# Performance work log

Measured on AMD Instinct MI355X. Metric: run time of the kernel, lower is better.

Reference implementation:

```python
import jax, jax.numpy as jnp
import numpy as np

B, K, S = 4096, 32, 6          # batch, n_neighbors, n_shifts
QD, H, NH = 512, 384, 6        # query_dim, hidden_dim, n_heads
HD = H // NH                   # head_dim
NR = 20                        # n_residue_types (table has NR+1 rows)
NBR_IN = S + S + 16 + 1 + 1    # neighbor_proj input dim = 30

def gelu(x):
    return jax.nn.gelu(x, approximate=False)

def setup_inputs():
    key = jax.random.key(0)
    ks = iter(jax.random.split(key, 64))
    def nrm(shape, scale=0.05):
        return jax.random.normal(next(ks), shape, dtype=jnp.float32) * scale
    inp = {}
    inp['query_encoding'] = jax.random.normal(next(ks), (B, QD), dtype=jnp.float32)
    inp['query_residue_code'] = jax.random.randint(next(ks), (B,), 0, NR + 1).astype(jnp.int32)
    inp['query_observed_shifts'] = jax.random.normal(next(ks), (B, S), dtype=jnp.float32)
    inp['query_shift_masks'] = (jax.random.uniform(next(ks), (B, S)) < 0.8).astype(jnp.float32)
    inp['retrieved_shifts'] = jax.random.normal(next(ks), (B, K, S), dtype=jnp.float32)
    inp['retrieved_shift_masks'] = jax.random.uniform(next(ks), (B, K, S)) < 0.8
    inp['retrieved_residue_codes'] = jax.random.randint(next(ks), (B, K), 0, NR + 1).astype(jnp.int32)
    inp['retrieved_distances'] = jax.random.uniform(next(ks), (B, K), dtype=jnp.float32)
    inp['retrieved_valid'] = jax.random.uniform(next(ks), (B, K)) < 0.9
    # parameters (buffers + weights). rc_table kept finite (no NaN rows sampled).
    inp['rc_table'] = nrm((NR + 1, S), 1.0)
    inp['W_qp'] = nrm((QD, H)); inp['b_qp'] = jnp.zeros((H,))
    inp['E_res'] = nrm((NR + 1, 16))
    inp['W_np'] = nrm((NBR_IN, H)); inp['b_np'] = jnp.zeros((H,))
    inp['W_aq'] = nrm((H, H)); inp['b_aq'] = jnp.zeros((H,))
    inp['W_ak'] = nrm((H, H)); inp['b_ak'] = jnp.zeros((H,))
    inp['W_av'] = nrm((H, H)); inp['b_av'] = jnp.zeros((H,))
    inp['W_ss1'] = nrm((2 * S, H // 2)); inp['b_ss1'] = jnp.zeros((H // 2,))
    inp['W_ss2'] = nrm((H // 2, NH)); inp['b_ss2'] = jnp.zeros((NH,))
    inp['W_cp1'] = nrm((H, H)); inp['b_cp1'] = jnp.zeros((H,))
    inp['W_cp2'] = nrm((H, H)); inp['b_cp2'] = jnp.zeros((H,))
    inp['W_sw1'] = nrm((H, H)); inp['b_sw1'] = jnp.zeros((H,))
    inp['W_sw2'] = nrm((H, S)); inp['b_sw2'] = jnp.zeros((S,))
    inp['E_trust'] = nrm((NR + 1, 32))
    inp['W_tq'] = nrm((QD, H)); inp['b_tq'] = jnp.zeros((H,))
    inp['W_tc'] = nrm((H + 32 + 4, H)); inp['b_tc'] = jnp.zeros((H,))
    inp['W_tp1'] = nrm((H + 4, H // 2)); inp['b_tp1'] = jnp.zeros((H // 2,))
    inp['W_tp2'] = nrm((H // 2, 1)); inp['b_tp2'] = jnp.zeros((1,))
    inp['shift_scale'] = jnp.ones((S,)); inp['fallback_shift'] = jnp.zeros((S,))
    inp['fallback_context'] = jnp.zeros((H,))
    return inp

def _forward(p):
    eps = 1e-8
    qcode = p['query_residue_code']; rcodes = p['retrieved_residue_codes']
    smask = p['retrieved_shift_masks']; valid = p['retrieved_valid']
    dist = p['retrieved_distances']; rc = p['rc_table']
    # --- RC correction: corrected = RC[query] + (shift - RC[retrieved]) ---
    qidx = jnp.clip(qcode, 0, rc.shape[0] - 1)
    ridx = jnp.clip(rcodes, 0, rc.shape[0] - 1)
    rc_q = rc[qidx][:, None, :]            # (B,1,S)
    rc_r = rc[ridx]                         # (B,K,S)
    corrected = rc_q + (p['retrieved_shifts'] - rc_r)
    rc_valid = (~jnp.isnan(rc_q)) & (~jnp.isnan(rc_r))
    corrected = jnp.where(rc_valid, corrected, p['retrieved_shifts'])
    shifts = jnp.where(smask, corrected, p['retrieved_shifts'])  # (B,K,S)
    any_valid = valid.any(axis=1)                                # (B,)
    same_type = (rcodes == qcode[:, None]).astype(jnp.float32)   # (B,K)
    # --- projections ---
    q = gelu(p['query_encoding'] @ p['W_qp'] + p['b_qp'])        # (B,H)
    res_emb = p['E_res'][rcodes]                                 # (B,K,16)
    nbr = jnp.concatenate([shifts, smask.astype(jnp.float32), res_emb,
                           dist[..., None], same_type[..., None]], axis=-1)
    kv = gelu(nbr @ p['W_np'] + p['b_np'])                       # (B,K,H)
    # --- multi-head cross attention (single query token) ---
    Qh = (q @ p['W_aq'] + p['b_aq']).reshape(B, NH, HD)
    Kh = (kv @ p['W_ak'] + p['b_ak']).reshape(B, K, NH, HD)
    Vh = (kv @ p['W_av'] + p['b_av']).reshape(B, K, NH, HD)
    scores = jnp.einsum('bhd,bkhd->bhk', Qh, Kh) * (HD ** -0.5)  # (B,NH,K)
    sdiff = jnp.concatenate([
        (p['query_observed_shifts'][:, None, :] - shifts) * p['query_shift_masks'][:, None, :],
        jnp.broadcast_to(p['query_shift_masks'][:, None, :], (B, K, S))], axis=-1)
    bias = gelu(sdiff @ p['W_ss1'] + p['b_ss1']) @ p['W_ss2'] + p['b_ss2']  # (B,K,NH)
    scores = scores + jnp.transpose(bias, (0, 2, 1))
    # if nothing valid, unmask slot 0 (matches torch all_masked fixup)
    valid_eff = valid | ((~any_valid)[:, None] & (jnp.arange(K) == 0)[None, :])
    scores = jnp.where(valid_eff[:, None, :], scores, -10000.0)
    w = jax.nn.softmax(scores, axis=-1)
    attn_out = jnp.einsum('bhk,bkhd->bhd', w, Vh).reshape(B, H)
    ctx = gelu(attn_out @ p['W_cp1'] + p['b_cp1']) @ p['W_cp2'] + p['b_cp2']
    ctx = jnp.where(any_valid[:, None], ctx, p['fallback_context'][None, :])
    # --- shift transfer ---
    swb = gelu(attn_out @ p['W_sw1'] + p['b_sw1']) @ p['W_sw2'] + p['b_sw2']  # (B,S)
    weights = dist[..., None] + same_type[..., None] * 0.5 + swb[:, None, :] * 0.1  # (B,K,S)
    valid_mask = valid[..., None] & smask
    weights = jnp.where(valid_mask, weights, -10000.0)
    weights = jax.nn.softmax(weights, axis=1)
    transferred = jnp.sum(weights * shifts, axis=1) * p['shift_scale']
    transferred = jnp.where(any_valid[:, None], transferred, p['fallback_shift'][None, :])
    # --- trust statistics (no grad in original) ---
    vm = valid_mask.astype(jnp.float32)
    cnt = vm.sum(axis=1)                                         # (B,S)
    cov = cnt / (K + eps)
    mean = (shifts * vm).sum(axis=1) / (cnt + eps)
    var = (((shifts - mean[:, None, :]) ** 2) * vm).sum(axis=1) / (cnt + eps)
    var_n = jnp.clip(jnp.log1p(var), 0.0, 5.0) / 5.0
    mdist = (dist[..., None] * vm).sum(axis=1) / (cnt + eps)
    stp = (same_type[..., None] * vm).sum(axis=1) / (cnt + eps)
    per_stats = jax.lax.stop_gradient(jnp.stack([cov, var_n, mdist, stp], axis=-1))  # (B,S,4)
    vf = valid.astype(jnp.float32)
    n_valid = vf.sum(axis=1, keepdims=True) / K
    n_same = (same_type * vf).sum(axis=1, keepdims=True) / K
    dmask = jnp.where(valid, dist, 0.0)
    gmean = dmask.sum(axis=1, keepdims=True) / (vf.sum(axis=1, keepdims=True) + eps)
    gmax = dmask.max(axis=1, keepdims=True)
    gstats = jax.lax.stop_gradient(jnp.concatenate([gmean, gmax, n_valid, n_same], axis=-1))  # (B,4)
    # --- trust head ---
    qre = p['E_trust'][qcode]                                    # (B,32)
    tq = gelu(p['query_encoding'] @ p['W_tq'] + p['b_tq'])
    tc = gelu(jnp.concatenate([tq, qre, gstats], axis=-1) @ p['W_tc'] + p['b_tc'])  # (B,H)
    tin = jnp.concatenate([jnp.broadcast_to(tc[:, None, :], (B, S, H)), per_stats], axis=-1)
    trust = jax.nn.sigmoid(gelu(tin @ p['W_tp1'] + p['b_tp1']) @ p['W_tp2'] + p['b_tp2'])[..., 0]
    return ctx, transferred, trust

def reference(query_encoding, query_residue_code, query_observed_shifts, query_shift_masks,
              retrieved_shifts, retrieved_shift_masks, retrieved_residue_codes,
              retrieved_distances, retrieved_valid, rc_table,
              W_qp, b_qp, E_res, W_np, b_np, W_aq, b_aq, W_ak, b_ak, W_av, b_av,
              W_ss1, b_ss1, W_ss2, b_ss2, W_cp1, b_cp1, W_cp2, b_cp2,
              W_sw1, b_sw1, W_sw2, b_sw2, E_trust, W_tq, b_tq, W_tc, b_tc,
              W_tp1, b_tp1, W_tp2, b_tp2, shift_scale, fallback_shift, fallback_context):
    return _forward(dict(locals()))
```

## Files before the change

kernel.cpp:

```cpp
#include <hip/hip_runtime.h>

typedef unsigned short u16;
typedef unsigned int u32;
typedef __attribute__((ext_vector_type(8))) short bf16x8;
typedef __attribute__((ext_vector_type(4))) float f32x4;

__device__ __forceinline__ float fs(float f) {
    return (f == f && fabsf(f) < 1e30f) ? f : 0.f;
}
__device__ __forceinline__ float fin(float v) {
    return (v == v && fabsf(v) < 1e30f) ? v : 555.0f;
}
__device__ __forceinline__ u16 f2b(float f) {
    union { float f; unsigned int i; } w; w.f = f;
    unsigned int r = w.i + 0x7FFFu + ((w.i >> 16) & 1u);
    return (u16)(r >> 16);
}
__device__ __forceinline__ float b2f(u16 b) {
    union { unsigned int i; float f; } w; w.i = ((unsigned int)b) << 16;
    return w.f;
}
__device__ __forceinline__ float gelu_f(float x) {
    return 0.5f * x * (1.0f + erff(x * 0.70710678118654752440f));
}

__global__ void fill_kernel(float* __restrict__ out, int n, float val) {
    int i = blockIdx.x * 256 + threadIdx.x;
    if (i < n) out[i] = val;
}

struct CvtSrcs { const float* p[14]; };

__global__ void k_cvt_all(CvtSrcs sp, u16* __restrict__ w) {
    int id = blockIdx.x * 256 + threadIdx.x;
    if (id >= 3640448) return;
    if (id < 2097152) { w[id] = f2b(fs(sp.p[0][id])); return; }
    if (id >= 2637824 && id < 2785280) { w[id] = f2b(fs(sp.p[4][id - 2637824])); return; }
    const float* src; int local, K, N, Kp;
    if (id < 2293760)      { src = sp.p[1];  local = id - 2097152; K = 512; N = 384; Kp = 512; }
    else if (id < 2490368) { src = sp.p[2];  local = id - 2293760; K = 512; N = 384; Kp = 512; }
    else if (id < 2637824) { src = sp.p[3];  local = id - 2490368; K = 384; N = 384; Kp = 384; }
    else if (id < 2932736) { src = sp.p[5];  local = id - 2785280; K = 384; N = 384; Kp = 384; }
    else if (id < 3080192) { src = sp.p[6];  local = id - 2932736; K = 384; N = 384; Kp = 384; }
    else if (id < 3227648) { src = sp.p[7];  local = id - 3080192; K = 384; N = 384; Kp = 384; }
    else if (id < 3375104) { src = sp.p[8];  local = id - 3227648; K = 384; N = 384; Kp = 384; }
    else if (id < 3547136) { src = sp.p[9];  local = id - 3375104; K = 420; N = 384; Kp = 448; }
    else if (id < 3620864) { src = sp.p[10]; local = id - 3547136; K = 384; N = 192; Kp = 384; }
    else if (id < 3633152) { src = sp.p[11]; local = id - 3620864; K = 30;  N = 384; Kp = 32;  }
    else if (id < 3634304) { src = sp.p[12]; local = id - 3633152; K = 192; N = 6;   Kp = 192; }
    else                   { src = sp.p[13]; local = id - 3634304; K = 12;  N = 192; Kp = 32;  }
    int n = local / Kp, k = local - n * Kp;
    w[id] = (k < K) ? f2b(fs(src[(size_t)k * N + n])) : (u16)0;
}

__global__ void k_prep(const float* __restrict__ rshift, const int* __restrict__ rsmask,
                       const int* __restrict__ qcode, const int* __restrict__ rcodes,
                       const float* __restrict__ rdist, const float* __restrict__ rc_table,
                       const float* __restrict__ E_res,
                       float* __restrict__ nbr, int NBc)
{
    int gk = blockIdx.x * 256 + threadIdx.x;
    if (gk >= NBc) return;
    int b = gk >> 5;
    int qc = qcode[b], rc = rcodes[gk];
    int qi = min(max(qc, 0), 20), ri = min(max(rc, 0), 20);
    float dist = fs(rdist[gk]);
    float same = (rc == qc) ? 1.f : 0.f;
    float* nr = nbr + (size_t)gk * 30;
    for (int s = 0; s < 6; s++) {
        float rs = fs(rshift[gk * 6 + s]);
        bool m = rsmask[gk * 6 + s] != 0;
        float rq = rc_table[qi * 6 + s];
        float rr = rc_table[ri * 6 + s];
        bool rcv = (rq == rq) && (rr == rr) && fabsf(rq) < 1e30f && fabsf(rr) < 1e30f;
        float sh = (m && rcv) ? (rq + rs - rr) : rs;
        nr[s] = sh;
        nr[6 + s] = m ? 1.f : 0.f;
    }
    for (int j = 0; j < 16; j++) nr[12 + j] = fs(E_res[ri * 16 + j]);
    nr[28] = dist;
    nr[29] = same;
}

__global__ void k_stats_w(const float* __restrict__ nbr, const int* __restrict__ rvalid,
                          float* __restrict__ pst, float* __restrict__ gst,
                          float* __restrict__ anyv, int BCc)
{
    int wid = (blockIdx.x * 256 + threadIdx.x) >> 6;
    int lane = threadIdx.x & 63;
    if (wid >= BCc * 4) return;
    int b = wid >> 2, sub = wid & 3;
    if (sub < 3) {
        int s = sub * 2 + (lane >> 5), k = lane & 31;
        const float* nr = nbr + (size_t)(b * 32 + k) * 30;
        float vf = (rvalid[b * 32 + k] != 0) ? 1.f : 0.f;
        float vm = vf * nr[6 + s];
        float shv = nr[s], dist = nr[28], same = nr[29];
        float cnt = vm, msum = shv * vm, mdist = dist * vm, mst = same * vm;
#pragma unroll
        for (int m = 1; m <= 16; m <<= 1) {
            cnt += __shfl_xor(cnt, m);
            msum += __shfl_xor(msum, m);
            mdist += __shfl_xor(mdist, m);
            mst += __shfl_xor(mst, m);
        }
        float inv = 1.f / (cnt + 1e-8f);
        float mean = msum * inv;
        float dv = shv - mean;
        float var = dv * dv * vm;
#pragma unroll
        for (int m = 1; m <= 16; m <<= 1) var += __shfl_xor(var, m);
        var *= inv;
        if (k == 0) {
            float* p = pst + (size_t)b * 24 + s * 4;
            p[0] = cnt * (1.f / 32.f);
            p[1] = fminf(fmaxf(log1pf(var), 0.f), 5.f) * 0.2f;
            p[2] = mdist * inv;
            p[3] = mst * inv;
        }
    } else {
        int k = lane & 31;
        float svf = 0.f, sdm = 0.f, mdm = -1e30f, ssm = 0.f;
        if (lane < 32) {
            const float* nr = nbr + (size_t)(b * 32 + k) * 30;
            float vf = (rvalid[b * 32 + k] != 0) ? 1.f : 0.f;
            float dm = vf * nr[28];
            svf = vf; sdm = dm; mdm = dm; ssm = vf * nr[29];
        }
#pragma unroll
        for (int m = 1; m <= 32; m <<= 1) {
            svf += __shfl_xor(svf, m);
            sdm += __shfl_xor(sdm, m);
            mdm = fmaxf(mdm, __shfl_xor(mdm, m));
            ssm += __shfl_xor(ssm, m);
        }
        if (lane == 0) {
            float* g = gst + (size_t)b * 4;
            g[0] = sdm / (svf + 1e-8f);
            g[1] = mdm;
            g[2] = svf * (1.f / 32.f);
            g[3] = ssm * (1.f / 32.f);
            anyv[b] = (svf > 0.f) ? 1.f : 0.f;
        }
    }
}

template <int ACT, bool OUTF, bool OUTB>
__device__ __forceinline__ void gemm_body128(
    const u16* __restrict__ A, int lda,
    const u16* __restrict__ BT, int ldb,
    const float* __restrict__ bias, const float* __restrict__ bias1,
    float* __restrict__ Cf, u16* __restrict__ Cb, int ldc,
    int K, int m0, int n0)
{
    __shared__ u16 As[128 * 72];
    __shared__ u16 Bs[64 * 72];
    const int t = threadIdx.x;
    const int lane = t & 63, wave = t >> 6;
    const int wm = (wave & 1) << 6, wn = (wave >> 1) << 5;
    const int frm = lane & 15, frq = lane >> 4;
    const int r0 = t >> 3, c0 = (t & 7) << 3;
    const f32x4 z = {0.f, 0.f, 0.f, 0.f};
    f32x4 acc[4][2] = {{z, z}, {z, z}, {z, z}, {z, z}};
    for (int k0 = 0; k0 < K; k0 += 64) {
#pragma unroll
        for (int i = 0; i < 4; i++)
            *(bf16x8*)&As[(r0 + 32 * i) * 72 + c0] =
                *(const bf16x8*)&A[(size_t)(m0 + r0 + 32 * i) * lda + k0 + c0];
#pragma unroll
        for (int i = 0; i < 2; i++)
            *(bf16x8*)&Bs[(r0 + 32 * i) * 72 + c0] =
                *(const bf16x8*)&BT[(size_t)(n0 + r0 + 32 * i) * ldb + k0 + c0];
        __syncthreads();
#pragma unroll
        for (int kk = 0; kk < 2; kk++) {
            const int fo = (kk << 5) + (frq << 3);
            bf16x8 b0 = *(const bf16x8*)&Bs[(wn + frm) * 72 + fo];
            bf16x8 b1 = *(const bf16x8*)&Bs[(wn + 16 + frm) * 72 + fo];
#pragma unroll
            for (int mi = 0; mi < 4; mi++) {
                bf16x8 a = *(const bf16x8*)&As[(wm + (mi << 4) + frm) * 72 + fo];
                acc[mi][0] = __builtin_amdgcn_mfma_f32_16x16x32_bf16(a, b0, acc[mi][0], 0, 0, 0);
                acc[mi][1] = __builtin_amdgcn_mfma_f32_16x16x32_bf16(a, b1, acc[mi][1], 0, 0, 0);
            }
        }
        __syncthreads();
    }
#pragma unroll
    for (int mi = 0; mi < 4; mi++) {
#pragma unroll
        for (int ni = 0; ni < 2; ni++) {
            int col = n0 + wn + (ni << 4) + frm;
            float bv = 0.f;
            if (bias) {
                if (bias1 && col >= 384) bv = fs(bias1[col - 384]);
                else bv = fs(bias[col]);
            }
#pragma unroll
            for (int r = 0; r < 4; r++) {
                int row = m0 + wm + (mi << 4) + (frq << 2) + r;
                float v = acc[mi][ni][r] + bv;
                if (ACT == 1) v = gelu_f(v);
                if (OUTF) Cf[(size_t)row * ldc + col] = v;
                if (OUTB) Cb[(size_t)row * ldc + col] = f2b(v);
            }
        }
    }
}

template <int ACT, bool OUTF, bool OUTB>
__global__ __launch_bounds__(256) void k_gemm_bb(
    const u16* __restrict__ A, int lda, const u16* __restrict__ BT, int ldb,
    const float* __restrict__ bias, float* __restrict__ Cf, u16* __restrict__ Cb,
    int ldc, int K)
{
    gemm_body128<ACT, OUTF, OUTB>(A, lda, BT, ldb, bias, nullptr, Cf, Cb, ldc, K,
                                  blockIdx.y << 7, blockIdx.x << 6);
}

template <int ACT>
__global__ __launch_bounds__(256) void k_gemm_bb2(
    const u16* __restrict__ A, int lda, const u16* __restrict__ BT, int ldb,
    const float* __restrict__ bias0, const float* __restrict__ bias1,
    u16* __restrict__ Cb, int ldc, int K)
{
    gemm_body128<ACT, false, true>(A, lda, BT, ldb, bias0, bias1, nullptr, Cb, ldc, K,
                                   blockIdx.y << 7, blockIdx.x << 6);
}

__global__ __launch_bounds__(256) void k_gemm_ctx(
    const u16* __restrict__ A, int lda, const u16* __restrict__ BT, int ldb,
    const float* __restrict__ bias, const float* __restrict__ anyv,
    const float* __restrict__ fctx, float* __restrict__ outp, int ldc, int K)
{
    __shared__ u16 As[128 * 72];
    __shared__ u16 Bs[64 * 72];
    const int t = threadIdx.x;
    const int lane = t & 63, wave = t >> 6;
    const int m0 = blockIdx.y << 7, n0 = blockIdx.x << 6;
    const int wm = (wave & 1) << 6, wn = (wave >> 1) << 5;
    const int frm = lane & 15, frq = lane >> 4;
    const int r0 = t >> 3, c0 = (t & 7) << 3;
    const f32x4 z = {0.f, 0.f, 0.f, 0.f};
    f32x4 acc[4][2] = {{z, z}, {z, z}, {z, z}, {z, z}};
    for (int k0 = 0; k0 < K; k0 += 64) {
#pragma unroll
        for (int i = 0; i < 4; i++)
            *(bf16x8*)&As[(r0 + 32 * i) * 72 + c0] =
                *(const bf16x8*)&A[(size_t)(m0 + r0 + 32 * i) * lda + k0 + c0];
#pragma unroll
        for (int i = 0; i < 2; i++)
            *(bf16x8*)&Bs[(r0 + 32 * i) * 72 + c0] =
                *(const bf16x8*)&BT[(size_t)(n0 + r0 + 32 * i) * ldb + k0 + c0];
        __syncthreads();
#pragma unroll
        for (int kk = 0; kk < 2; kk++) {
            const int fo = (kk << 5) + (frq << 3);
            bf16x8 b0 = *(const bf16x8*)&Bs[(wn + frm) * 72 + fo];
            bf16x8 b1 = *(const bf16x8*)&Bs[(wn + 16 + frm) * 72 + fo];
#pragma unroll
            for (int mi = 0; mi < 4; mi++) {
                bf16x8 a = *(const bf16x8*)&As[(wm + (mi << 4) + frm) * 72 + fo];
                acc[mi][0] = __builtin_amdgcn_mfma_f32_16x16x32_bf16(a, b0, acc[mi][0], 0, 0, 0);
                acc[mi][1] = __builtin_amdgcn_mfma_f32_16x16x32_bf16(a, b1, acc[mi][1], 0, 0, 0);
            }
        }
        __syncthreads();
    }
#pragma unroll
    for (int mi = 0; mi < 4; mi++) {
#pragma unroll
        for (int ni = 0; ni < 2; ni++) {
            int col = n0 + wn + (ni << 4) + frm;
            float bv = fs(bias[col]);
            float fv = fs(fctx[col]);
#pragma unroll
            for (int r = 0; r < 4; r++) {
                int row = m0 + wm + (mi << 4) + (frq << 2) + r;
                float v = acc[mi][ni][r] + bv;
                v = (anyv[row] > 0.f) ? v : fv;
                outp[(size_t)row * ldc + col] = fin(v);
            }
        }
    }
}

__global__ __launch_bounds__(256) void k_gemm_tc(
    const u16* __restrict__ qtqb, const int* __restrict__ qcode,
    const float* __restrict__ Etr, const float* __restrict__ gst,
    const u16* __restrict__ BT, const float* __restrict__ bias,
    u16* __restrict__ Cb)
{
    __shared__ u16 As[128 * 72];
    __shared__ u16 Bs[64 * 72];
    const int t = threadIdx.x;
    const int lane = t & 63, wave = t >> 6;
    const int m0 = blockIdx.y << 7, n0 = blockIdx.x << 6;
    const int wm = (wave & 1) << 6, wn = (wave >> 1) << 5;
    const int frm = lane & 15, frq = lane >> 4;
    const int r0 = t >> 3, c0 = (t & 7) << 3;
    const f32x4 z = {0.f, 0.f, 0.f, 0.f};
    f32x4 acc[4][2] = {{z, z}, {z, z}, {z, z}, {z, z}};
    for (int k0 = 0; k0 < 448; k0 += 64) {
        if (k0 < 384) {
#pragma unroll
            for (int i = 0; i < 4; i++)
                *(bf16x8*)&As[(r0 + 32 * i) * 72 + c0] =
                    *(const bf16x8*)&qtqb[(size_t)(m0 + r0 + 32 * i) * 768 + 384 + k0 + c0];
        } else {
#pragma unroll
            for (int i = 0; i < 4; i++) {
                int row = m0 + r0 + 32 * i;
                int qi = min(max(qcode[row], 0), 20);
#pragma unroll
                for (int j = 0; j < 8; j++) {
                    int col = k0 + c0 + j;
                    u16 v;
                    if (col < 416) v = f2b(fs(Etr[qi * 32 + (col - 384)]));
                    else if (col < 420) v = f2b(gst[(size_t)row * 4 + (col - 416)]);
                    else v = (u16)0;
                    As[(r0 + 32 * i) * 72 + c0 + j] = v;
                }
            }
        }
#pragma unroll
        for (int i = 0; i < 2; i++)
            *(bf16x8*)&Bs[(r0 + 32 * i) * 72 + c0] =
                *(const bf16x8*)&BT[(size_t)(n0 + r0 + 32 * i) * 448 + k0 + c0];
        __syncthreads();
#pragma unroll
        for (int kk = 0; kk < 2; kk++) {
            const int fo = (kk << 5) + (frq << 3);
            bf16x8 b0 = *(const bf16x8*)&Bs[(wn + frm) * 72 + fo];
            bf16x8 b1 = *(const bf16x8*)&Bs[(wn + 16 + frm) * 72 + fo];
#pragma unroll
            for (int mi = 0; mi < 4; mi++) {
                bf16x8 a = *(const bf16x8*)&As[(wm + (mi << 4) + frm) * 72 + fo];
                acc[mi][0] = __builtin_amdgcn_mfma_f32_16x16x32_bf16(a, b0, acc[mi][0], 0, 0, 0);
                acc[mi][1] = __builtin_amdgcn_mfma_f32_16x16x32_bf16(a, b1, acc[mi][1], 0, 0, 0);
            }
        }
        __syncthreads();
    }
#pragma unroll
    for (int mi = 0; mi < 4; mi++) {
#pragma unroll
        for (int ni = 0; ni < 2; ni++) {
            int col = n0 + wn + (ni << 4) + frm;
            float bv = fs(bias[col]);
#pragma unroll
            for (int r = 0; r < 4; r++) {
                int row = m0 + wm + (mi << 4) + (frq << 2) + r;
                Cb[(size_t)row * 384 + col] = f2b(gelu_f(acc[mi][ni][r] + bv));
            }
        }
    }
}

__global__ __launch_bounds__(256) void k_qp_loop(
    const u16* __restrict__ Qhb, const u16* __restrict__ WakB,
    const float* __restrict__ bak, u16* __restrict__ Qpb, float* __restrict__ qkb)
{
    __shared__ u16 As[64 * 72];
    __shared__ u16 Bs[64 * 72];
    const int t = threadIdx.x;
    const int lane = t & 63, wave = t >> 6;
    const int m0 = blockIdx.x << 6, hd = blockIdx.y;
    const int wm = (wave & 1) << 5, wn = (wave >> 1) << 5;
    const int frm = lane & 15, frq = lane >> 4;
    const int r0 = t >> 3, c0 = (t & 7) << 3;
    const f32x4 z = {0.f, 0.f, 0.f, 0.f};
    *(bf16x8*)&As[r0 * 72 + c0]        = *(const bf16x8*)&Qhb[(size_t)(m0 + r0) * 384 + hd * 64 + c0];
    *(bf16x8*)&As[(r0 + 32) * 72 + c0] = *(const bf16x8*)&Qhb[(size_t)(m0 + r0 + 32) * 384 + hd * 64 + c0];
    __syncthreads();
    {
        int r = t >> 2, p = t & 3;
        float acc = 0.f;
#pragma unroll
        for (int i = 0; i < 16; i++) {
            int d = p * 16 + i;
            acc += b2f(As[r * 72 + d]) * fs(bak[hd * 64 + d]);
        }
        acc += __shfl_xor(acc, 1);
        acc += __shfl_xor(acc, 2);
        if (p == 0) qkb[(m0 + r) * 6 + hd] = acc;
    }
    for (int nt = 0; nt < 6; nt++) {
        *(bf16x8*)&Bs[r0 * 72 + c0]        = *(const bf16x8*)&WakB[(size_t)(nt * 64 + r0) * 384 + hd * 64 + c0];
        *(bf16x8*)&Bs[(r0 + 32) * 72 + c0] = *(const bf16x8*)&WakB[(size_t)(nt * 64 + r0 + 32) * 384 + hd * 64 + c0];
        __syncthreads();
        f32x4 acc[2][2] = {{z, z}, {z, z}};
#pragma unroll
        for (int kk = 0; kk < 2; kk++) {
            const int fo = (kk << 5) + (frq << 3);
            bf16x8 a0 = *(const bf16x8*)&As[(wm + frm) * 72 + fo];
            bf16x8 a1 = *(const bf16x8*)&As[(wm + 16 + frm) * 72 + fo];
            bf16x8 b0 = *(const bf16x8*)&Bs[(wn + frm) * 72 + fo];
            bf16x8 b1 = *(const bf16x8*)&Bs[(wn + 16 + frm) * 72 + fo];
            acc[0][0] = __builtin_amdgcn_mfma_f32_16x16x32_bf16(a0, b0, acc[0][0], 0, 0, 0);
            acc[0][1] = __builtin_amdgcn_mfma_f32_16x16x32_bf16(a0, b1, acc[0][1], 0, 0, 0);
            acc[1][0] = __builtin_amdgcn_mfma_f32_16x16x32_bf16(a1, b0, acc[1][0], 0, 0, 0);
            acc[1][1] = __builtin_amdgcn_mfma_f32_16x16x32_bf16(a1, b1, acc[1][1], 0, 0, 0);
        }
#pragma unroll
        for (int mi = 0; mi < 2; mi++) {
#pragma unroll
            for (int ni = 0; ni < 2; ni++) {
                int col = nt * 64 + wn + (ni << 4) + frm;
#pragma unroll
                for (int r = 0; r < 4; r++) {
                    int row = m0 + wm + (mi << 4) + (frq << 2) + r;
                    Qpb[(size_t)row * 2304 + hd * 384 + col] = f2b(acc[mi][ni][r]);
                }
            }
        }
        __syncthreads();
    }
}

__global__ __launch_bounds__(256) void k_attnout_bb(
    const u16* __restrict__ vmsb, const u16* __restrict__ WavT,
    const float* __restrict__ bav, u16* __restrict__ attnb)
{
    int hd = blockIdx.x;
    gemm_body128<0, false, true>(vmsb + hd * 384, 2304, WavT + (size_t)hd * 64 * 384, 384,
                                 bav + hd * 64, nullptr, nullptr, attnb + hd * 64, 384, 384,
                                 blockIdx.y << 7, 0);
}

__global__ __launch_bounds__(384) void k_attnblk(
    const float* __restrict__ nbr, const u16* __restrict__ WnpT,
    const float* __restrict__ bnp, const u16* __restrict__ Qpb,
    const float* __restrict__ qkb,
    const float* __restrict__ qobs, const float* __restrict__ qmask,
    const u16* __restrict__ Wss1T, const float* __restrict__ bss1,
    const u16* __restrict__ Wss2T, const float* __restrict__ bss2,
    const int* __restrict__ rvalid, const float* __restrict__ anyv,
    u16* __restrict__ vmsb)
{
    __shared__ u16 kvsb[32 * 392];
    __shared__ u16 qSb[6 * 392];
    __shared__ u16 hidSb[32 * 200];
    __shared__ u16 sdS[32 * 32];
    __shared__ float wsx[192];
    __shared__ float bsS[32 * 8];
    __shared__ float uSf[512];
    u16* aS = (u16*)uSf;
    float* sS = uSf;
    const int b = blockIdx.x;
    const int t = threadIdx.x;
    const int lane = t & 63, wave = t >> 6;
    const int frm = lane & 15, frq = lane >> 4;
    for (int i = t; i < 1152; i += 384) {
        int h = i / 192, k2 = i - h * 192;
        ((u32*)qSb)[h * 196 + k2] = ((const u32*)(Qpb + (size_t)b * 2304))[i];
    }
    {
        const float* nr = nbr + (size_t)b * 960;
        for (int i = t; i < 1024; i += 384) {
            int r = i >> 5, cc = i & 31;
            aS[r * 32 + cc] = (cc < 30) ? f2b(nr[r * 30 + cc]) : (u16)0;
        }
        if (t < 32) {
            const float* nr2 = nr + t * 30;
#pragma unroll
            for (int s = 0; s < 6; s++) {
                float qm = fs(qmask[b * 6 + s]);
                sdS[t * 32 + s] = f2b((fs(qobs[b * 6 + s]) - nr2[s]) * qm);
                sdS[t * 32 + 6 + s] = f2b(qm);
            }
#pragma unroll
            for (int j = 12; j < 32; j++) sdS[t * 32 + j] = (u16)0;
        }
    }
    __syncthreads();
    {
        bf16x8 a0 = *(const bf16x8*)&aS[frm * 32 + (frq << 3)];
        bf16x8 a1 = *(const bf16x8*)&aS[(16 + frm) * 32 + (frq << 3)];
        const f32x4 z = {0.f, 0.f, 0.f, 0.f};
        f32x4 acc0[4] = {z, z, z, z};
        f32x4 acc1[4] = {z, z, z, z};
#pragma unroll
        for (int ct = 0; ct < 4; ct++) {
            int col = (wave << 6) + (ct << 4) + frm;
            bf16x8 bf = *(const bf16x8*)&WnpT[col * 32 + (frq << 3)];
            acc0[ct] = __builtin_amdgcn_mfma_f32_16x16x32_bf16(a0, bf, acc0[ct], 0, 0, 0);
            acc1[ct] = __builtin_amdgcn_mfma_f32_16x16x32_bf16(a1, bf, acc1[ct], 0, 0, 0);
        }
#pragma unroll
        for (int ct = 0; ct < 4; ct++) {
            int col = (wave << 6) + (ct << 4) + frm;
            float bb = fs(bnp[col]);
#pragma unroll
            for (int r = 0; r < 4; r++) {
                int row0 = (frq << 2) + r;
                kvsb[row0 * 392 + col] = f2b(gelu_f(acc0[ct][r] + bb));
                kvsb[(row0 + 16) * 392 + col] = f2b(gelu_f(acc1[ct][r] + bb));
            }
        }
        bf16x8 sa0 = *(const bf16x8*)&sdS[frm * 32 + (frq << 3)];
        bf16x8 sa1 = *(const bf16x8*)&sdS[(16 + frm) * 32 + (frq << 3)];
#pragma unroll
        for (int ct = 0; ct < 2; ct++) {
            int col = (wave << 5) + (ct << 4) + frm;
            bf16x8 bf = *(const bf16x8*)&Wss1T[col * 32 + (frq << 3)];
            f32x4 d0 = __builtin_amdgcn_mfma_f32_16x16x32_bf16(sa0, bf, z, 0, 0, 0);
            f32x4 d1 = __builtin_amdgcn_mfma_f32_16x16x32_bf16(sa1, bf, z, 0, 0, 0);
            float bb = fs(bss1[col]);
#pragma unroll
            for (int r = 0; r < 4; r++) {
                int k0r = (frq << 2) + r;
                hidSb[k0r * 200 + col] = f2b(gelu_f(d0[r] + bb));
                hidSb[(k0r + 16) * 200 + col] = f2b(gelu_f(d1[r] + bb));
            }
        }
    }
    __syncthreads();
    if (wave < 2) {
        f32x4 accs = {0.f, 0.f, 0.f, 0.f};
#pragma unroll
        for (int ks = 0; ks < 12; ks++) {
            bf16x8 af = *(const bf16x8*)&kvsb[((wave << 4) + frm) * 392 + (ks << 5) + (frq << 3)];
            int hh = (frm < 6) ? frm : 0;
            bf16x8 bf = *(const bf16x8*)&qSb[hh * 392 + (ks << 5) + (frq << 3)];
            accs = __builtin_amdgcn_mfma_f32_16x16x32_bf16(af, bf, accs, 0, 0, 0);
        }
        if (frm < 6) {
#pragma unroll
            for (int r = 0; r < 4; r++)
                sS[((wave << 4) + (frq << 2) + r) * 8 + frm] = accs[r];
        }
    } else if (wave < 4) {
        int w2 = wave - 2;
        f32x4 accb = {0.f, 0.f, 0.f, 0.f};
#pragma unroll
        for (int ks = 0; ks < 6; ks++) {
            bf16x8 a = *(const bf16x8*)&hidSb[((w2 << 4) + frm) * 200 + (ks << 5) + (frq << 3)];
            bf16x8 bf = *(const bf16x8*)&Wss2T[(frm < 6 ? frm : 0) * 192 + (ks << 5) + (frq << 3)];
            accb = __builtin_amdgcn_mfma_f32_16x16x32_bf16(a, bf, accb, 0, 0, 0);
        }
        if (frm < 6) {
            float bb = fs(bss2[frm]);
#pragma unroll
            for (int r = 0; r < 4; r++)
                bsS[((w2 << 4) + (frq << 2) + r) * 8 + frm] = accb[r] + bb;
        }
    }
    __syncthreads();
    if (t < 192) {
        int h = t >> 5, k = t & 31;
        float s = (sS[k * 8 + h] + qkb[b * 6 + h]) * 0.125f + bsS[k * 8 + h];
        bool ve = (rvalid[b * 32 + k] != 0) || (anyv[b] == 0.f && k == 0);
        s = ve ? s : -10000.f;
        float mx = s;
        mx = fmaxf(mx, __shfl_xor(mx, 1));
        mx = fmaxf(mx, __shfl_xor(mx, 2));
        mx = fmaxf(mx, __shfl_xor(mx, 4));
        mx = fmaxf(mx, __shfl_xor(mx, 8));
        mx = fmaxf(mx, __shfl_xor(mx, 16));
        float e = expf(s - mx);
        float sum = e;
        sum += __shfl_xor(sum, 1);
        sum += __shfl_xor(sum, 2);
        sum += __shfl_xor(sum, 4);
        sum += __shfl_xor(sum, 8);
        sum += __shfl_xor(sum, 16);
        wsx[h * 32 + k] = e / sum;
    }
    __syncthreads();
    {
        float a0 = 0.f, a1 = 0.f, a2 = 0.f, a3 = 0.f, a4 = 0.f, a5 = 0.f;
        for (int k = 0; k < 32; k++) {
            float kvv = b2f(kvsb[k * 392 + t]);
            a0 += wsx[k] * kvv;
            a1 += wsx[32 + k] * kvv;
            a2 += wsx[64 + k] * kvv;
            a3 += wsx[96 + k] * kvv;
            a4 += wsx[128 + k] * kvv;
            a5 += wsx[160 + k] * kvv;
        }
        u16* vp = vmsb + (size_t)b * 2304;
        vp[t] = f2b(a0);
        vp[384 + t] = f2b(a1);
        vp[768 + t] = f2b(a2);
        vp[1152 + t] = f2b(a3);
        vp[1536 + t] = f2b(a4);
        vp[1920 + t] = f2b(a5);
    }
}

__global__ void k_swb_w(const u16* __restrict__ hs1b, const float* __restrict__ Wsw2,
                        const float* __restrict__ bsw2, float* __restrict__ swb, int BCc)
{
    int wid = (blockIdx.x * 256 + threadIdx.x) >> 6;
    int lane = threadIdx.x & 63;
    if (wid >= BCc * 6) return;
    int b = wid / 6, s = wid - b * 6;
    float acc = 0.f;
#pragma unroll
    for (int i = 0; i < 6; i++) {
        int n = lane + 64 * i;
        acc += b2f(hs1b[(size_t)b * 768 + 384 + n]) * fs(Wsw2[n * 6 + s]);
    }
#pragma unroll
    for (int m = 1; m <= 32; m <<= 1) acc += __shfl_xor(acc, m);
    if (lane == 0) swb[b * 6 + s] = acc + fs(bsw2[s]);
}

__global__ void k_tail_w(const float* __restrict__ tcp, const float* __restrict__ pst,
                         const float* __restrict__ Wtp1, const float* __restrict__ Wtp2,
                         const float* __restrict__ btp2, float* __restrict__ outT,
                         const float* __restrict__ nbr, const int* __restrict__ rsmask,
                         const int* __restrict__ rvalid, const float* __restrict__ swb,
                         const float* __restrict__ anyv, const float* __restrict__ sscale,
                         const float* __restrict__ fshift, float* __restrict__ outX, int BCc)
{
    int wid = (blockIdx.x * 256 + threadIdx.x) >> 6;
    int lane = threadIdx.x & 63;
    if (wid >= BCc * 9) return;
    int b = wid / 9, sub = wid - b * 9;
    if (sub < 6) {
        int s = sub;
        const float* ps = pst + (size_t)b * 24 + s * 4;
        float p0 = ps[0], p1 = ps[1], p2 = ps[2], p3 = ps[3];
        float acc = 0.f;
#pragma unroll
        for (int i = 0; i < 3; i++) {
            int j = lane + 64 * i;
            float pre = tcp[(size_t)b * 192 + j];
            pre += p0 * fs(Wtp1[(size_t)384 * 192 + j]);
            pre += p1 * fs(Wtp1[(size_t)385 * 192 + j]);
            pre += p2 * fs(Wtp1[(size_t)386 * 192 + j]);
            pre += p3 * fs(Wtp1[(size_t)387 * 192 + j]);
            acc += gelu_f(pre) * fs(Wtp2[j]);
        }
#pragma unroll
        for (int m = 1; m <= 32; m <<= 1) acc += __shfl_xor(acc, m);
        if (lane == 0) {
            float tv = 1.f / (1.f + expf(-(acc + fs(btp2[0]))));
            outT[b * 6 + s] = fin(tv);
        }
    } else {
        int s2 = sub - 6;
        int s = s2 * 2 + (lane >> 5), k = lane & 31;
        if (anyv[b] <= 0.f) {
            if (k == 0) outX[b * 6 + s] = fin(fs(fshift[s]));
            return;
        }
        int gk = b * 32 + k;
        const float* nr = nbr + (size_t)gk * 30;
        float wb = swb[b * 6 + s] * 0.1f;
        bool m = (rvalid[gk] != 0) && (rsmask[gk * 6 + s] != 0);
        float wv = m ? (nr[28] + nr[29] * 0.5f + wb) : -10000.f;
        float mx = wv;
#pragma unroll
        for (int mm = 1; mm <= 16; mm <<= 1) mx = fmaxf(mx, __shfl_xor(mx, mm));
        float e = expf(wv - mx);
        float num = e * nr[s], den = e;
#pragma unroll
        for (int mm = 1; mm <= 16; mm <<= 1) {
            num += __shfl_xor(num, mm);
            den += __shfl_xor(den, mm);
        }
        if (k == 0) outX[b * 6 + s] = fin((num / den) * fs(sscale[s]));
    }
}

#define L1(total) <<<((total) + 255) / 256, 256, 0, stream>>>
#define LW(nwaves) <<<(((nwaves) * 64) + 255) / 256, 256, 0, stream>>>

extern "C" void kernel_launch(void* const* d_in, const int* in_sizes, int n_in,
                              void* d_out, int out_size, void* d_ws, size_t ws_size,
                              hipStream_t stream)
{
    float* out = (float*)d_out;

    static const int EXP[45] = {
        2097152, 4096, 24576, 24576, 786432, 786432, 131072, 131072, 131072, 126,
        196608, 384, 336, 11520, 384, 147456, 384, 147456, 384, 147456, 384,
        2304, 192, 1152, 6, 147456, 384, 147456, 384, 147456, 384, 2304, 6,
        672, 196608, 384, 161280, 384, 74496, 192, 192, 1, 6, 6, 384
    };
    if (n_in != 45) {
        fill_kernel L1(out_size)(out, out_size, 580.0f);
        return;
    }
    for (int i = 0; i < 45; i++) {
        if (in_sizes[i] != EXP[i]) {
            fill_kernel L1(out_size)(out, out_size, 600.0f + 4.0f * i);
            return;
        }
    }

    const float* i_qe    = (const float*)d_in[0];
    const int*   i_qcode = (const int*)d_in[1];
    const float* i_qobs  = (const float*)d_in[2];
    const float* i_qmask = (const float*)d_in[3];
    const float* i_rshift= (const float*)d_in[4];
    const int*   i_rsmask= (const int*)d_in[5];
    const int*   i_rcodes= (const int*)d_in[6];
    const float* i_rdist = (const float*)d_in[7];
    const int*   i_rvalid= (const int*)d_in[8];
    const float* i_rc    = (const float*)d_in[9];
    const float* i_Wqp   = (const float*)d_in[10];
    const float* i_bqp   = (const float*)d_in[11];
    const float* i_Eres  = (const float*)d_in[12];
    const float* i_Wnp   = (const float*)d_in[13];
    const float* i_bnp   = (const float*)d_in[14];
    const float* i_Waq   = (const float*)d_in[15];
    const float* i_baq   = (const float*)d_in[16];
    const float* i_Wak   = (const float*)d_in[17];
    const float* i_bak   = (const float*)d_in[18];
    const float* i_Wav   = (const float*)d_in[19];
    const float* i_bav   = (const float*)d_in[20];
    const float* i_Wss1  = (const float*)d_in[21];
    const float* i_bss1  = (const float*)d_in[22];
    const float* i_Wss2  = (const float*)d_in[23];
    const float* i_bss2  = (const float*)d_in[24];
    const float* i_Wcp1  = (const float*)d_in[25];
    const float* i_bcp1  = (const float*)d_in[26];
    const float* i_Wcp2  = (const float*)d_in[27];
    const float* i_bcp2  = (const float*)d_in[28];
    const float* i_Wsw1  = (const float*)d_in[29];
    const float* i_bsw1  = (const float*)d_in[30];
    const float* i_Wsw2  = (const float*)d_in[31];
    const float* i_bsw2  = (const float*)d_in[32];
    const float* i_Etr   = (const float*)d_in[33];
    const float* i_Wtq   = (const float*)d_in[34];
    const float* i_btq   = (const float*)d_in[35];
    const float* i_Wtc   = (const float*)d_in[36];
    const float* i_btc   = (const float*)d_in[37];
    const float* i_Wtp1  = (const float*)d_in[38];
    const float* i_btp1  = (const float*)d_in[39];
    const float* i_Wtp2  = (const float*)d_in[40];
    const float* i_btp2  = (const float*)d_in[41];
    const float* i_sscale= (const float*)d_in[42];
    const float* i_fshift= (const float*)d_in[43];
    const float* i_fctx  = (const float*)d_in[44];

    auto layoutBytes = [](int bc) -> size_t {
        auto al = [](size_t x) { return (x + 255) & ~(size_t)255; };
        size_t off = 0;
        off += al(3640448ull * 2);
        size_t nb = (size_t)bc * 32;
        off += al(nb * 30 * 4);
        off += al((size_t)bc * 192 * 4);
        off += al((size_t)bc * 2304 * 2) * 2;
        off += al((size_t)bc * 768 * 2) * 2;
        off += al((size_t)bc * 384 * 2) * 3;
        off += al((size_t)bc * 6 * 4) * 2 + al((size_t)bc * 24 * 4)
             + al((size_t)bc * 4 * 4) + al((size_t)bc * 4);
        return off;
    };
    const int cand[6] = {4096, 2048, 1024, 512, 256, 128};
    int BCc = 128;
    for (int i = 0; i < 6; i++) {
        if (layoutBytes(cand[i]) <= ws_size) { BCc = cand[i]; break; }
    }
    const int NBc = BCc * 32;

    char* wsb = (char*)d_ws;
    size_t off = 0;
    auto allocB = [&](size_t bytes) -> void* {
        void* p = (void*)(wsb + off);
        off = (off + bytes + 255) & ~(size_t)255;
        return p;
    };
    u16* wsW = (u16*)allocB(3640448ull * 2);
    u16* qeb   = wsW;
    u16* WqtqT = wsW + 2097152;
    u16* WaqT  = wsW + 2490368;
    u16* WakB  = wsW + 2637824;
    u16* WavT  = wsW + 2785280;
    u16* Wcp2T = wsW + 2932736;
    u16* Whs1T = wsW + 3080192;
    u16* WtcT  = wsW + 3375104;
    u16* Wtp1T = wsW + 3547136;
    u16* WnpT  = wsW + 3620864;
    u16* Wss2T = wsW + 3633152;
    u16* Wss1T = wsW + 3634304;
    float* nbr   = (float*)allocB((size_t)NBc * 30 * 4);
    float* tcpf  = (float*)allocB((size_t)BCc * 192 * 4);
    u16*   Qpb   = (u16*)allocB((size_t)BCc * 2304 * 2);
    u16*   vmsb  = (u16*)allocB((size_t)BCc * 2304 * 2);
    u16*   qtqb  = (u16*)allocB((size_t)BCc * 768 * 2);
    u16*   hs1b  = (u16*)allocB((size_t)BCc * 768 * 2);
    u16*   Qhb   = (u16*)allocB((size_t)BCc * 384 * 2);
    u16*   attnb = (u16*)allocB((size_t)BCc * 384 * 2);
    u16*   tcb   = (u16*)allocB((size_t)BCc * 384 * 2);
    float* swbf  = (float*)allocB((size_t)BCc * 6 * 4);
    float* qkbf  = (float*)allocB((size_t)BCc * 6 * 4);
    float* pstf  = (float*)allocB((size_t)BCc * 24 * 4);
    float* gstf  = (float*)allocB((size_t)BCc * 4 * 4);
    float* anyf  = (float*)allocB((size_t)BCc * 4);

    if (off > ws_size) {
        fill_kernel L1(out_size)(out, out_size, 1000.0f);
        return;
    }

    CvtSrcs sp;
    sp.p[0] = i_qe;  sp.p[1] = i_Wqp;  sp.p[2] = i_Wtq;  sp.p[3] = i_Waq;
    sp.p[4] = i_Wak; sp.p[5] = i_Wav;  sp.p[6] = i_Wcp2; sp.p[7] = i_Wcp1;
    sp.p[8] = i_Wsw1; sp.p[9] = i_Wtc; sp.p[10] = i_Wtp1; sp.p[11] = i_Wnp;
    sp.p[12] = i_Wss2; sp.p[13] = i_Wss1;
    k_cvt_all L1(3640448)(sp, wsW);

    for (int c = 0; c < 4096 / BCc; c++) {
        const size_t B0 = (size_t)c * BCc;
        const int MB = BCc / 128;
        const dim3 g6(6, MB), g3(3, MB), g12(12, MB), gao(6, MB);
        const dim3 gqp(BCc / 64, 6);
        k_prep L1(NBc)(i_rshift + B0 * 192, i_rsmask + B0 * 192, i_qcode + B0,
                       i_rcodes + B0 * 32, i_rdist + B0 * 32, i_rc, i_Eres, nbr, NBc);
        k_stats_w LW(BCc * 4)(nbr, i_rvalid + B0 * 32, pstf, gstf, anyf, BCc);
        k_gemm_bb2<1><<<g12, 256, 0, stream>>>(
            qeb + B0 * 512, 512, WqtqT, 512, i_bqp, i_btq, qtqb, 768, 512);
        k_gemm_bb<0, false, true><<<g6, 256, 0, stream>>>(
            qtqb, 768, WaqT, 384, i_baq, nullptr, Qhb, 384, 384);
        k_qp_loop<<<gqp, 256, 0, stream>>>(Qhb, WakB, i_bak, Qpb, qkbf);
        k_attnblk<<<BCc, 384, 0, stream>>>(nbr, WnpT, i_bnp, Qpb, qkbf,
                                           i_qobs + B0 * 6, i_qmask + B0 * 6,
                                           Wss1T, i_bss1, Wss2T, i_bss2,
                                           i_rvalid + B0 * 32, anyf, vmsb);
        k_attnout_bb<<<gao, 256, 0, stream>>>(vmsb, WavT, i_bav, attnb);
        k_gemm_bb2<1><<<g12, 256, 0, stream>>>(
            attnb, 384, Whs1T, 384, i_bcp1, i_bsw1, hs1b, 768, 384);
        k_gemm_ctx<<<g6, 256, 0, stream>>>(
            hs1b, 768, Wcp2T, 384, i_bcp2, anyf, i_fctx, out + B0 * 384, 384, 384);
        k_swb_w LW(BCc * 6)(hs1b, i_Wsw2, i_bsw2, swbf, BCc);
        k_gemm_tc<<<g6, 256, 0, stream>>>(
            qtqb, i_qcode + B0, i_Etr, gstf, WtcT, i_btc, tcb);
        k_gemm_bb<0, true, false><<<g3, 256, 0, stream>>>(
            tcb, 384, Wtp1T, 384, i_btp1, tcpf, nullptr, 192, 384);
        k_tail_w LW(BCc * 9)(tcpf, pstf, i_Wtp1, i_Wtp2, i_btp2,
                             out + (size_t)4096 * 390 + B0 * 6,
                             nbr, i_rsmask + B0 * 192, i_rvalid + B0 * 32, swbf, anyf,
                             i_sscale, i_fshift, out + (size_t)4096 * 384 + B0 * 6, BCc);
    }
}
```

Before: 394.2 us.

## Merge independent per-chunk kernels into combined launches and trim attention shared memory

```diff
diff --git a/kernel.cpp b/kernel.cpp
--- a/kernel.cpp
+++ b/kernel.cpp
@@ -53,14 +53,261 @@
     w[id] = (k < K) ? f2b(fs(src[(size_t)k * N + n])) : (u16)0;
 }
 
-__global__ void k_prep(const float* __restrict__ rshift, const int* __restrict__ rsmask,
-                       const int* __restrict__ qcode, const int* __restrict__ rcodes,
-                       const float* __restrict__ rdist, const float* __restrict__ rc_table,
-                       const float* __restrict__ E_res,
-                       float* __restrict__ nbr, int NBc)
-{
-    int gk = blockIdx.x * 256 + threadIdx.x;
-    if (gk >= NBc) return;
+
+template <int ACT, bool OUTF, bool OUTB>
+__device__ void gemm_body128(
+    u16* As, u16* Bs,
+    const u16* __restrict__ A, int lda,
+    const u16* __restrict__ BT, int ldb,
+    const float* __restrict__ bias, const float* __restrict__ bias1,
+    float* __restrict__ Cf, u16* __restrict__ Cb, int ldc,
+    int K, int m0, int n0)
+{
+    const int t = threadIdx.x;
+    const int lane = t & 63, wave = t >> 6;
+    const int wm = (wave & 1) << 6, wn = (wave >> 1) << 5;
+    const int frm = lane & 15, frq = lane >> 4;
+    const int r0 = t >> 3, c0 = (t & 7) << 3;
+    const f32x4 z = {0.f, 0.f, 0.f, 0.f};
+    f32x4 acc[4][2] = {{z, z}, {z, z}, {z, z}, {z, z}};
+    for (int k0 = 0; k0 < K; k0 += 64) {
+#pragma unroll
+        for (int i = 0; i < 4; i++)
+            *(bf16x8*)&As[(r0 + 32 * i) * 72 + c0] =
+                *(const bf16x8*)&A[(size_t)(m0 + r0 + 32 * i) * lda + k0 + c0];
+#pragma unroll
+        for (int i = 0; i < 2; i++)
+            *(bf16x8*)&Bs[(r0 + 32 * i) * 72 + c0] =
+                *(const bf16x8*)&BT[(size_t)(n0 + r0 + 32 * i) * ldb + k0 + c0];
+        __syncthreads();
+#pragma unroll
+        for (int kk = 0; kk < 2; kk++) {
+            const int fo = (kk << 5) + (frq << 3);
+            bf16x8 b0 = *(const bf16x8*)&Bs[(wn + frm) * 72 + fo];
+            bf16x8 b1 = *(const bf16x8*)&Bs[(wn + 16 + frm) * 72 + fo];
+#pragma unroll
+            for (int mi = 0; mi < 4; mi++) {
+                bf16x8 a = *(const bf16x8*)&As[(wm + (mi << 4) + frm) * 72 + fo];
+                acc[mi][0] = __builtin_amdgcn_mfma_f32_16x16x32_bf16(a, b0, acc[mi][0], 0, 0, 0);
+                acc[mi][1] = __builtin_amdgcn_mfma_f32_16x16x32_bf16(a, b1, acc[mi][1], 0, 0, 0);
+            }
+        }
+        __syncthreads();
+    }
+#pragma unroll
+    for (int mi = 0; mi < 4; mi++) {
+#pragma unroll
+        for (int ni = 0; ni < 2; ni++) {
+            int col = n0 + wn + (ni << 4) + frm;
+            float bv = 0.f;
+            if (bias) {
+                if (bias1 && col >= 384) bv = fs(bias1[col - 384]);
+                else bv = fs(bias[col]);
+            }
+#pragma unroll
+            for (int r = 0; r < 4; r++) {
+                int row = m0 + wm + (mi << 4) + (frq << 2) + r;
+                float v = acc[mi][ni][r] + bv;
+                if (ACT == 1) v = gelu_f(v);
+                if (OUTF) Cf[(size_t)row * ldc + col] = v;
+                if (OUTB) Cb[(size_t)row * ldc + col] = f2b(v);
+            }
+        }
+    }
+}
+
+__device__ void gemm_ctx_body(
+    u16* As, u16* Bs,
+    const u16* __restrict__ A, const u16* __restrict__ BT,
+    const float* __restrict__ bias, const float* __restrict__ anyv,
+    const float* __restrict__ fctx, float* __restrict__ outp,
+    int m0, int n0)
+{
+    const int t = threadIdx.x;
+    const int lane = t & 63, wave = t >> 6;
+    const int wm = (wave & 1) << 6, wn = (wave >> 1) << 5;
+    const int frm = lane & 15, frq = lane >> 4;
+    const int r0 = t >> 3, c0 = (t & 7) << 3;
+    const f32x4 z = {0.f, 0.f, 0.f, 0.f};
+    f32x4 acc[4][2] = {{z, z}, {z, z}, {z, z}, {z, z}};
+    for (int k0 = 0; k0 < 384; k0 += 64) {
+#pragma unroll
+        for (int i = 0; i < 4; i++)
+            *(bf16x8*)&As[(r0 + 32 * i) * 72 + c0] =
+                *(const bf16x8*)&A[(size_t)(m0 + r0 + 32 * i) * 768 + k0 + c0];
+#pragma unroll
+        for (int i = 0; i < 2; i++)
+            *(bf16x8*)&Bs[(r0 + 32 * i) * 72 + c0] =
+                *(const bf16x8*)&BT[(size_t)(n0 + r0 + 32 * i) * 384 + k0 + c0];
+        __syncthreads();
+#pragma unroll
+        for (int kk = 0; kk < 2; kk++) {
+            const int fo = (kk << 5) + (frq << 3);
+            bf16x8 b0 = *(const bf16x8*)&Bs[(wn + frm) * 72 + fo];
+            bf16x8 b1 = *(const bf16x8*)&Bs[(wn + 16 + frm) * 72 + fo];
+#pragma unroll
+            for (int mi = 0; mi < 4; mi++) {
+                bf16x8 a = *(const bf16x8*)&As[(wm + (mi << 4) + frm) * 72 + fo];
+                acc[mi][0] = __builtin_amdgcn_mfma_f32_16x16x32_bf16(a, b0, acc[mi][0], 0, 0, 0);
+                acc[mi][1] = __builtin_amdgcn_mfma_f32_16x16x32_bf16(a, b1, acc[mi][1], 0, 0, 0);
+            }
+        }
+        __syncthreads();
+    }
+#pragma unroll
+    for (int mi = 0; mi < 4; mi++) {
+#pragma unroll
+        for (int ni = 0; ni < 2; ni++) {
+            int col = n0 + wn + (ni << 4) + frm;
+            float bv = fs(bias[col]);
+            float fv = fs(fctx[col]);
+#pragma unroll
+            for (int r = 0; r < 4; r++) {
+                int row = m0 + wm + (mi << 4) + (frq << 2) + r;
+                float v = acc[mi][ni][r] + bv;
+                v = (anyv[row] > 0.f) ? v : fv;
+                outp[(size_t)row * 384 + col] = fin(v);
+            }
+        }
+    }
+}
+
+__device__ void gemm_tc_body(
+    u16* As, u16* Bs,
+    const u16* __restrict__ qtqb, const int* __restrict__ qcode,
+    const float* __restrict__ Etr, const float* __restrict__ gst,
+    const u16* __restrict__ BT, const float* __restrict__ bias,
+    u16* __restrict__ Cb, int m0, int n0)
+{
+    const int t = threadIdx.x;
+    const int lane = t & 63, wave = t >> 6;
+    const int wm = (wave & 1) << 6, wn = (wave >> 1) << 5;
+    const int frm = lane & 15, frq = lane >> 4;
+    const int r0 = t >> 3, c0 = (t & 7) << 3;
+    const f32x4 z = {0.f, 0.f, 0.f, 0.f};
+    f32x4 acc[4][2] = {{z, z}, {z, z}, {z, z}, {z, z}};
+    for (int k0 = 0; k0 < 448; k0 += 64) {
+        if (k0 < 384) {
+#pragma unroll
+            for (int i = 0; i < 4; i++)
+                *(bf16x8*)&As[(r0 + 32 * i) * 72 + c0] =
+                    *(const bf16x8*)&qtqb[(size_t)(m0 + r0 + 32 * i) * 768 + 384 + k0 + c0];
+        } else {
+#pragma unroll
+            for (int i = 0; i < 4; i++) {
+                int row = m0 + r0 + 32 * i;
+                int qi = min(max(qcode[row], 0), 20);
+#pragma unroll
+                for (int j = 0; j < 8; j++) {
+                    int col = k0 + c0 + j;
+                    u16 v;
+                    if (col < 416) v = f2b(fs(Etr[qi * 32 + (col - 384)]));
+                    else if (col < 420) v = f2b(gst[(size_t)row * 4 + (col - 416)]);
+                    else v = (u16)0;
+                    As[(r0 + 32 * i) * 72 + c0 + j] = v;
+                }
+            }
+        }
+#pragma unroll
+        for (int i = 0; i < 2; i++)
+            *(bf16x8*)&Bs[(r0 + 32 * i) * 72 + c0] =
+                *(const bf16x8*)&BT[(size_t)(n0 + r0 + 32 * i) * 448 + k0 + c0];
+        __syncthreads();
+#pragma unroll
+        for (int kk = 0; kk < 2; kk++) {
+            const int fo = (kk << 5) + (frq << 3);
+            bf16x8 b0 = *(const bf16x8*)&Bs[(wn + frm) * 72 + fo];
+            bf16x8 b1 = *(const bf16x8*)&Bs[(wn + 16 + frm) * 72 + fo];
+#pragma unroll
+            for (int mi = 0; mi < 4; mi++) {
+                bf16x8 a = *(const bf16x8*)&As[(wm + (mi << 4) + frm) * 72 + fo];
+                acc[mi][0] = __builtin_amdgcn_mfma_f32_16x16x32_bf16(a, b0, acc[mi][0], 0, 0, 0);
+                acc[mi][1] = __builtin_amdgcn_mfma_f32_16x16x32_bf16(a, b1, acc[mi][1], 0, 0, 0);
+            }
+        }
+        __syncthreads();
+    }
+#pragma unroll
+    for (int mi = 0; mi < 4; mi++) {
+#pragma unroll
+        for (int ni = 0; ni < 2; ni++) {
+            int col = n0 + wn + (ni << 4) + frm;
+            float bv = fs(bias[col]);
+#pragma unroll
+            for (int r = 0; r < 4; r++) {
+                int row = m0 + wm + (mi << 4) + (frq << 2) + r;
+                Cb[(size_t)row * 384 + col] = f2b(gelu_f(acc[mi][ni][r] + bv));
+            }
+        }
+    }
+}
+
+__device__ void qp_body(
+    u16* As, u16* Bs,
+    const u16* __restrict__ Qhb, const u16* __restrict__ WakB,
+    const float* __restrict__ bak, u16* __restrict__ Qpb, float* __restrict__ qkb,
+    int m0, int hd)
+{
+    const int t = threadIdx.x;
+    const int lane = t & 63, wave = t >> 6;
+    const int wm = (wave & 1) << 5, wn = (wave >> 1) << 5;
+    const int frm = lane & 15, frq = lane >> 4;
+    const int r0 = t >> 3, c0 = (t & 7) << 3;
+    const f32x4 z = {0.f, 0.f, 0.f, 0.f};
+    *(bf16x8*)&As[r0 * 72 + c0]        = *(const bf16x8*)&Qhb[(size_t)(m0 + r0) * 384 + hd * 64 + c0];
+    *(bf16x8*)&As[(r0 + 32) * 72 + c0] = *(const bf16x8*)&Qhb[(size_t)(m0 + r0 + 32) * 384 + hd * 64 + c0];
+    __syncthreads();
+    {
+        int r = t >> 2, p = t & 3;
+        float acc = 0.f;
+#pragma unroll
+        for (int i = 0; i < 16; i++) {
+            int d = p * 16 + i;
+            acc += b2f(As[r * 72 + d]) * fs(bak[hd * 64 + d]);
+        }
+        acc += __shfl_xor(acc, 1);
+        acc += __shfl_xor(acc, 2);
+        if (p == 0) qkb[(m0 + r) * 6 + hd] = acc;
+    }
+    for (int nt = 0; nt < 6; nt++) {
+        *(bf16x8*)&Bs[r0 * 72 + c0]        = *(const bf16x8*)&WakB[(size_t)(nt * 64 + r0) * 384 + hd * 64 + c0];
+        *(bf16x8*)&Bs[(r0 + 32) * 72 + c0] = *(const bf16x8*)&WakB[(size_t)(nt * 64 + r0 + 32) * 384 + hd * 64 + c0];
+        __syncthreads();
+        f32x4 acc[2][2] = {{z, z}, {z, z}};
+#pragma unroll
+        for (int kk = 0; kk < 2; kk++) {
+            const int fo = (kk << 5) + (frq << 3);
+            bf16x8 a0 = *(const bf16x8*)&As[(wm + frm) * 72 + fo];
+            bf16x8 a1 = *(const bf16x8*)&As[(wm + 16 + frm) * 72 + fo];
+            bf16x8 b0 = *(const bf16x8*)&Bs[(wn + frm) * 72 + fo];
+            bf16x8 b1 = *(const bf16x8*)&Bs[(wn + 16 + frm) * 72 + fo];
+            acc[0][0] = __builtin_amdgcn_mfma_f32_16x16x32_bf16(a0, b0, acc[0][0], 0, 0, 0);
+            acc[0][1] = __builtin_amdgcn_mfma_f32_16x16x32_bf16(a0, b1, acc[0][1], 0, 0, 0);
+            acc[1][0] = __builtin_amdgcn_mfma_f32_16x16x32_bf16(a1, b0, acc[1][0], 0, 0, 0);
+            acc[1][1] = __builtin_amdgcn_mfma_f32_16x16x32_bf16(a1, b1, acc[1][1], 0, 0, 0);
+        }
+#pragma unroll
+        for (int mi = 0; mi < 2; mi++) {
+#pragma unroll
+            for (int ni = 0; ni < 2; ni++) {
+                int col = nt * 64 + wn + (ni << 4) + frm;
+#pragma unroll
+                for (int r = 0; r < 4; r++) {
+                    int row = m0 + wm + (mi << 4) + (frq << 2) + r;
+                    Qpb[(size_t)row * 2304 + hd * 384 + col] = f2b(acc[mi][ni][r]);
+                }
+            }
+        }
+        __syncthreads();
+    }
+}
+
+__device__ void prep_one(int gk,
+    const float* __restrict__ rshift, const int* __restrict__ rsmask,
+    const int* __restrict__ qcode, const int* __restrict__ rcodes,
+    const float* __restrict__ rdist, const float* __restrict__ rc_table,
+    const float* __restrict__ E_res, float* __restrict__ nbr)
+{
     int b = gk >> 5;
     int qc = qcode[b], rc = rcodes[gk];
     int qi = min(max(qc, 0), 20), ri = min(max(rc, 0), 20);
@@ -82,13 +329,10 @@
     nr[29] = same;
 }
 
-__global__ void k_stats_w(const float* __restrict__ nbr, const int* __restrict__ rvalid,
-                          float* __restrict__ pst, float* __restrict__ gst,
-                          float* __restrict__ anyv, int BCc)
-{
-    int wid = (blockIdx.x * 256 + threadIdx.x) >> 6;
-    int lane = threadIdx.x & 63;
-    if (wid >= BCc * 4) return;
+__device__ void stats_wave(int wid, int lane,
+    const float* __restrict__ nbr, const int* __restrict__ rvalid,
+    float* __restrict__ pst, float* __restrict__ gst, float* __restrict__ anyv)
+{
     int b = wid >> 2, sub = wid & 3;
     if (sub < 3) {
         int s = sub * 2 + (lane >> 5), k = lane & 31;
@@ -145,287 +389,145 @@
     }
 }
 
-template <int ACT, bool OUTF, bool OUTB>
-__device__ __forceinline__ void gemm_body128(
-    const u16* __restrict__ A, int lda,
-    const u16* __restrict__ BT, int ldb,
-    const float* __restrict__ bias, const float* __restrict__ bias1,
-    float* __restrict__ Cf, u16* __restrict__ Cb, int ldc,
-    int K, int m0, int n0)
+__device__ void swb_wave(int wid, int lane,
+    const u16* __restrict__ hs1b, const float* __restrict__ Wsw2,
+    const float* __restrict__ bsw2, float* __restrict__ swb)
+{
+    int b = wid / 6, s = wid - b * 6;
+    float acc = 0.f;
+#pragma unroll
+    for (int i = 0; i < 6; i++) {
+        int n = lane + 64 * i;
+        acc += b2f(hs1b[(size_t)b * 768 + 384 + n]) * fs(Wsw2[n * 6 + s]);
+    }
+#pragma unroll
+    for (int m = 1; m <= 32; m <<= 1) acc += __shfl_xor(acc, m);
+    if (lane == 0) swb[b * 6 + s] = acc + fs(bsw2[s]);
+}
+
+
+__global__ __launch_bounds__(256) void k_front(
+    const u16* __restrict__ A, const u16* __restrict__ BT,
+    const float* __restrict__ b0v, const float* __restrict__ b1v, u16* __restrict__ Cb,
+    const float* __restrict__ rshift, const int* __restrict__ rsmask,
+    const int* __restrict__ qcode, const int* __restrict__ rcodes,
+    const float* __restrict__ rdist, const float* __restrict__ rc_table,
+    const float* __restrict__ E_res, float* __restrict__ nbr, int MB, int NBc)
 {
     __shared__ u16 As[128 * 72];
     __shared__ u16 Bs[64 * 72];
-    const int t = threadIdx.x;
-    const int lane = t & 63, wave = t >> 6;
-    const int wm = (wave & 1) << 6, wn = (wave >> 1) << 5;
-    const int frm = lane & 15, frq = lane >> 4;
-    const int r0 = t >> 3, c0 = (t & 7) << 3;
-    const f32x4 z = {0.f, 0.f, 0.f, 0.f};
-    f32x4 acc[4][2] = {{z, z}, {z, z}, {z, z}, {z, z}};
-    for (int k0 = 0; k0 < K; k0 += 64) {
-#pragma unroll
-        for (int i = 0; i < 4; i++)
-            *(bf16x8*)&As[(r0 + 32 * i) * 72 + c0] =
-                *(const bf16x8*)&A[(size_t)(m0 + r0 + 32 * i) * lda + k0 + c0];
-#pragma unroll
-        for (int i = 0; i < 2; i++)
-            *(bf16x8*)&Bs[(r0 + 32 * i) * 72 + c0] =
-                *(const bf16x8*)&BT[(size_t)(n0 + r0 + 32 * i) * ldb + k0 + c0];
-        __syncthreads();
-#pragma unroll
-        for (int kk = 0; kk < 2; kk++) {
-            const int fo = (kk << 5) + (frq << 3);
-            bf16x8 b0 = *(const bf16x8*)&Bs[(wn + frm) * 72 + fo];
-            bf16x8 b1 = *(const bf16x8*)&Bs[(wn + 16 + frm) * 72 + fo];
-#pragma unroll
-            for (int mi = 0; mi < 4; mi++) {
-                bf16x8 a = *(const bf16x8*)&As[(wm + (mi << 4) + frm) * 72 + fo];
-                acc[mi][0] = __builtin_amdgcn_mfma_f32_16x16x32_bf16(a, b0, acc[mi][0], 0, 0, 0);
-                acc[mi][1] = __builtin_amdgcn_mfma_f32_16x16x32_bf16(a, b1, acc[mi][1], 0, 0, 0);
-            }
-        }
-        __syncthreads();
-    }
-#pragma unroll
-    for (int mi = 0; mi < 4; mi++) {
-#pragma unroll
-        for (int ni = 0; ni < 2; ni++) {
-            int col = n0 + wn + (ni << 4) + frm;
-            float bv = 0.f;
-            if (bias) {
-                if (bias1 && col >= 384) bv = fs(bias1[col - 384]);
-                else bv = fs(bias[col]);
-            }
-#pragma unroll
-            for (int r = 0; r < 4; r++) {
-                int row = m0 + wm + (mi << 4) + (frq << 2) + r;
-                float v = acc[mi][ni][r] + bv;
-                if (ACT == 1) v = gelu_f(v);
-                if (OUTF) Cf[(size_t)row * ldc + col] = v;
-                if (OUTB) Cb[(size_t)row * ldc + col] = f2b(v);
-            }
-        }
-    }
-}
-
-template <int ACT, bool OUTF, bool OUTB>
-__global__ __launch_bounds__(256) void k_gemm_bb(
-    const u16* __restrict__ A, int lda, const u16* __restrict__ BT, int ldb,
-    const float* __restrict__ bias, float* __restrict__ Cf, u16* __restrict__ Cb,
-    int ldc, int K)
-{
-    gemm_body128<ACT, OUTF, OUTB>(A, lda, BT, ldb, bias, nullptr, Cf, Cb, ldc, K,
-                                  blockIdx.y << 7, blockIdx.x << 6);
-}
-
-template <int ACT>
-__global__ __launch_bounds__(256) void k_gemm_bb2(
-    const u16* __restrict__ A, int lda, const u16* __restrict__ BT, int ldb,
-    const float* __restrict__ bias0, const float* __restrict__ bias1,
-    u16* __restrict__ Cb, int ldc, int K)
-{
-    gemm_body128<ACT, false, true>(A, lda, BT, ldb, bias0, bias1, nullptr, Cb, ldc, K,
-                                   blockIdx.y << 7, blockIdx.x << 6);
-}
-
-__global__ __launch_bounds__(256) void k_gemm_ctx(
-    const u16* __restrict__ A, int lda, const u16* __restrict__ BT, int ldb,
-    const float* __restrict__ bias, const float* __restrict__ anyv,
-    const float* __restrict__ fctx, float* __restrict__ outp, int ldc, int K)
+    int bid = blockIdx.x;
+    int G = 12 * MB;
+    if (bid < G) {
+        gemm_body128<1, false, true>(As, Bs, A, 512, BT, 512, b0v, b1v,
+                                     nullptr, Cb, 768, 512,
+                                     (bid / 12) << 7, (bid % 12) << 6);
+    } else {
+        int gk = (bid - G) * 256 + threadIdx.x;
+        if (gk < NBc)
+            prep_one(gk, rshift, rsmask, qcode, rcodes, rdist, rc_table, E_res, nbr);
+    }
+}
+
+__global__ __launch_bounds__(256) void k_mid(
+    const u16* __restrict__ qtqb, const u16* __restrict__ WaqT,
+    const float* __restrict__ baq, u16* __restrict__ Qhb,
+    const float* __restrict__ nbr, const int* __restrict__ rvalid,
+    float* __restrict__ pst, float* __restrict__ gst, float* __restrict__ anyv,
+    int MB, int BCc)
 {
     __shared__ u16 As[128 * 72];
     __shared__ u16 Bs[64 * 72];
-    const int t = threadIdx.x;
-    const int lane = t & 63, wave = t >> 6;
-    const int m0 = blockIdx.y << 7, n0 = blockIdx.x << 6;
-    const int wm = (wave & 1) << 6, wn = (wave >> 1) << 5;
-    const int frm = lane & 15, frq = lane >> 4;
-    const int r0 = t >> 3, c0 = (t & 7) << 3;
-    const f32x4 z = {0.f, 0.f, 0.f, 0.f};
-    f32x4 acc[4][2] = {{z, z}, {z, z}, {z, z}, {z, z}};
-    for (int k0 = 0; k0 < K; k0 += 64) {
-#pragma unroll
-        for (int i = 0; i < 4; i++)
-            *(bf16x8*)&As[(r0 + 32 * i) * 72 + c0] =
-                *(const bf16x8*)&A[(size_t)(m0 + r0 + 32 * i) * lda + k0 + c0];
-#pragma unroll
-        for (int i = 0; i < 2; i++)
-            *(bf16x8*)&Bs[(r0 + 32 * i) * 72 + c0] =
-                *(const bf16x8*)&BT[(size_t)(n0 + r0 + 32 * i) * ldb + k0 + c0];
-        __syncthreads();
-#pragma unroll
-        for (int kk = 0; kk < 2; kk++) {
-            const int fo = (kk << 5) + (frq << 3);
-            bf16x8 b0 = *(const bf16x8*)&Bs[(wn + frm) * 72 + fo];
-            bf16x8 b1 = *(const bf16x8*)&Bs[(wn + 16 + frm) * 72 + fo];
-#pragma unroll
-            for (int mi = 0; mi < 4; mi++) {
-                bf16x8 a = *(const bf16x8*)&As[(wm + (mi << 4) + frm) * 72 + fo];
-                acc[mi][0] = __builtin_amdgcn_mfma_f32_16x16x32_bf16(a, b0, acc[mi][0], 0, 0, 0);
-                acc[mi][1] = __builtin_amdgcn_mfma_f32_16x16x32_bf16(a, b1, acc[mi][1], 0, 0, 0);
-            }
-        }
-        __syncthreads();
-    }
-#pragma unroll
-    for (int mi = 0; mi < 4; mi++) {
-#pragma unroll
-        for (int ni = 0; ni < 2; ni++) {
-            int col = n0 + wn + (ni << 4) + frm;
-            float bv = fs(bias[col]);
-            float fv = fs(fctx[col]);
-#pragma unroll
-            for (int r = 0; r < 4; r++) {
-                int row = m0 + wm + (mi << 4) + (frq << 2) + r;
-                float v = acc[mi][ni][r] + bv;
-                v = (anyv[row] > 0.f) ? v : fv;
-                outp[(size_t)row * ldc + col] = fin(v);
-            }
-        }
-    }
-}
-
-__global__ __launch_bounds__(256) void k_gemm_tc(
+    int bid = blockIdx.x;
+    int G = 6 * MB;
+    if (bid < G) {
+        gemm_body128<0, false, true>(As, Bs, qtqb, 768, WaqT, 384, baq, nullptr,
+                                     nullptr, Qhb, 384, 384,
+                                     (bid / 6) << 7, (bid % 6) << 6);
+    } else {
+        int wid = (bid - G) * 4 + (threadIdx.x >> 6);
+        int lane = threadIdx.x & 63;
+        if (wid < BCc * 4) stats_wave(wid, lane, nbr, rvalid, pst, gst, anyv);
+    }
+}
+
+__global__ __launch_bounds__(256) void k_qptc(
+    const u16* __restrict__ Qhb, const u16* __restrict__ WakB,
+    const float* __restrict__ bak, u16* __restrict__ Qpb, float* __restrict__ qkb,
     const u16* __restrict__ qtqb, const int* __restrict__ qcode,
     const float* __restrict__ Etr, const float* __restrict__ gst,
-    const u16* __restrict__ BT, const float* __restrict__ bias,
-    u16* __restrict__ Cb)
+    const u16* __restrict__ WtcT, const float* __restrict__ btc, u16* __restrict__ tcb,
+    int BCc, int MB)
 {
     __shared__ u16 As[128 * 72];
     __shared__ u16 Bs[64 * 72];
-    const int t = threadIdx.x;
-    const int lane = t & 63, wave = t >> 6;
-    const int m0 = blockIdx.y << 7, n0 = blockIdx.x << 6;
-    const int wm = (wave & 1) << 6, wn = (wave >> 1) << 5;
-    const int frm = lane & 15, frq = lane >> 4;
-    const int r0 = t >> 3, c0 = (t & 7) << 3;
-    const f32x4 z = {0.f, 0.f, 0.f, 0.f};
-    f32x4 acc[4][2] = {{z, z}, {z, z}, {z, z}, {z, z}};
-    for (int k0 = 0; k0 < 448; k0 += 64) {
-        if (k0 < 384) {
-#pragma unroll
-            for (int i = 0; i < 4; i++)
-                *(bf16x8*)&As[(r0 + 32 * i) * 72 + c0] =
-                    *(const bf16x8*)&qtqb[(size_t)(m0 + r0 + 32 * i) * 768 + 384 + k0 + c0];
-        } else {
-#pragma unroll
-            for (int i = 0; i < 4; i++) {
-                int row = m0 + r0 + 32 * i;
-                int qi = min(max(qcode[row], 0), 20);
-#pragma unroll
-                for (int j = 0; j < 8; j++) {
-                    int col = k0 + c0 + j;
-                    u16 v;
-                    if (col < 416) v = f2b(fs(Etr[qi * 32 + (col - 384)]));
-                    else if (col < 420) v = f2b(gst[(size_t)row * 4 + (col - 416)]);
-                    else v = (u16)0;
-                    As[(r0 + 32 * i) * 72 + c0 + j] = v;
-                }
-            }
-        }
-#pragma unroll
-        for (int i = 0; i < 2; i++)
-            *(bf16x8*)&Bs[(r0 + 32 * i) * 72 + c0] =
-                *(const bf16x8*)&BT[(size_t)(n0 + r0 + 32 * i) * 448 + k0 + c0];
-        __syncthreads();
-#pragma unroll
-        for (int kk = 0; kk < 2; kk++) {
-            const int fo = (kk << 5) + (frq << 3);
-            bf16x8 b0 = *(const bf16x8*)&Bs[(wn + frm) * 72 + fo];
-            bf16x8 b1 = *(const bf16x8*)&Bs[(wn + 16 + frm) * 72 + fo];
-#pragma unroll
-            for (int mi = 0; mi < 4; mi++) {
-                bf16x8 a = *(const bf16x8*)&As[(wm + (mi << 4) + frm) * 72 + fo];
-                acc[mi][0] = __builtin_amdgcn_mfma_f32_16x16x32_bf16(a, b0, acc[mi][0], 0, 0, 0);
-                acc[mi][1] = __builtin_amdgcn_mfma_f32_16x16x32_bf16(a, b1, acc[mi][1], 0, 0, 0);
-            }
-        }
-        __syncthreads();
-    }
-#pragma unroll
-    for (int mi = 0; mi < 4; mi++) {
-#pragma unroll
-        for (int ni = 0; ni < 2; ni++) {
-            int col = n0 + wn + (ni << 4) + frm;
-            float bv = fs(bias[col]);
-#pragma unroll
-            for (int r = 0; r < 4; r++) {
-                int row = m0 + wm + (mi << 4) + (frq << 2) + r;
-                Cb[(size_t)row * 384 + col] = f2b(gelu_f(acc[mi][ni][r] + bv));
-            }
-        }
-    }
-}
-
-__global__ __launch_bounds__(256) void k_qp_loop(
-    const u16* __restrict__ Qhb, const u16* __restrict__ WakB,
-    const float* __restrict__ bak, u16* __restrict__ Qpb, float* __restrict__ qkb)
-{
-    __shared__ u16 As[64 * 72];
+    int bid = blockIdx.x;
+    int MQ = BCc / 64;
+    int G = MQ * 6;
+    if (bid < G) {
+        qp_body(As, Bs, Qhb, WakB, bak, Qpb, qkb, (bid % MQ) << 6, bid / MQ);
+    } else {
+        int b2 = bid - G;
+        gemm_tc_body(As, Bs, qtqb, qcode, Etr, gst, WtcT, btc, tcb,
+                     (b2 / 6) << 7, (b2 % 6) << 6);
+    }
+}
+
+__global__ __launch_bounds__(256) void k_aotp(
+    const u16* __restrict__ vmsb, const u16* __restrict__ WavT,
+    const float* __restrict__ bav, u16* __restrict__ attnb,
+    const u16* __restrict__ tcb, const u16* __restrict__ Wtp1T,
+    const float* __restrict__ btp1, float* __restrict__ tcpf, int MB)
+{
+    __shared__ u16 As[128 * 72];
     __shared__ u16 Bs[64 * 72];
-    const int t = threadIdx.x;
-    const int lane = t & 63, wave = t >> 6;
-    const int m0 = blockIdx.x << 6, hd = blockIdx.y;
-    const int wm = (wave & 1) << 5, wn = (wave >> 1) << 5;
-    const int frm = lane & 15, frq = lane >> 4;
-    const int r0 = t >> 3, c0 = (t & 7) << 3;
-    const f32x4 z = {0.f, 0.f, 0.f, 0.f};
-    *(bf16x8*)&As[r0 * 72 + c0]        = *(const bf16x8*)&Qhb[(size_t)(m0 + r0) * 384 + hd * 64 + c0];
-    *(bf16x8*)&As[(r0 + 32) * 72 + c0] = *(const bf16x8*)&Qhb[(size_t)(m0 + r0 + 32) * 384 + hd * 64 + c0];
-    __syncthreads();
-    {
-        int r = t >> 2, p = t & 3;
-        float acc = 0.f;
-#pragma unroll
-        for (int i = 0; i < 16; i++) {
-            int d = p * 16 + i;
-            acc += b2f(As[r * 72 + d]) * fs(bak[hd * 64 + d]);
-        }
-        acc += __shfl_xor(acc, 1);
-        acc += __shfl_xor(acc, 2);
-        if (p == 0) qkb[(m0 + r) * 6 + hd] = acc;
-    }
-    for (int nt = 0; nt < 6; nt++) {
-        *(bf16x8*)&Bs[r0 * 72 + c0]        = *(const bf16x8*)&WakB[(size_t)(nt * 64 + r0) * 384 + hd * 64 + c0];
-        *(bf16x8*)&Bs[(r0 + 32) * 72 + c0] = *(const bf16x8*)&WakB[(size_t)(nt * 64 + r0 + 32) * 384 + hd * 64 + c0];
-        __syncthreads();
-        f32x4 acc[2][2] = {{z, z}, {z, z}};
-#pragma unroll
-        for (int kk = 0; kk < 2; kk++) {
-            const int fo = (kk << 5) + (frq << 3);
-            bf16x8 a0 = *(const bf16x8*)&As[(wm + frm) * 72 + fo];
-            bf16x8 a1 = *(const bf16x8*)&As[(wm + 16 + frm) * 72 + fo];
-            bf16x8 b0 = *(const bf16x8*)&Bs[(wn + frm) * 72 + fo];
-            bf16x8 b1 = *(const bf16x8*)&Bs[(wn + 16 + frm) * 72 + fo];
-            acc[0][0] = __builtin_amdgcn_mfma_f32_16x16x32_bf16(a0, b0, acc[0][0], 0, 0, 0);
-            acc[0][1] = __builtin_amdgcn_mfma_f32_16x16x32_bf16(a0, b1, acc[0][1], 0, 0, 0);
-            acc[1][0] = __builtin_amdgcn_mfma_f32_16x16x32_bf16(a1, b0, acc[1][0], 0, 0, 0);
-            acc[1][1] = __builtin_amdgcn_mfma_f32_16x16x32_bf16(a1, b1, acc[1][1], 0, 0, 0);
-        }
-#pragma unroll
-        for (int mi = 0; mi < 2; mi++) {
-#pragma unroll
-            for (int ni = 0; ni < 2; ni++) {
-                int col = nt * 64 + wn + (ni << 4) + frm;
-#pragma unroll
-                for (int r = 0; r < 4; r++) {
-                    int row = m0 + wm + (mi << 4) + (frq << 2) + r;
-                    Qpb[(size_t)row * 2304 + hd * 384 + col] = f2b(acc[mi][ni][r]);
-                }
-            }
-        }
-        __syncthreads();
-    }
-}
-
-__global__ __launch_bounds__(256) void k_attnout_bb(
-    const u16* __restrict__ vmsb, const u16* __restrict__ WavT,
-    const float* __restrict__ bav, u16* __restrict__ attnb)
-{
-    int hd = blockIdx.x;
-    gemm_body128<0, false, true>(vmsb + hd * 384, 2304, WavT + (size_t)hd * 64 * 384, 384,
-                                 bav + hd * 64, nullptr, nullptr, attnb + hd * 64, 384, 384,
-                                 blockIdx.y << 7, 0);
+    int bid = blockIdx.x;
+    int G = 6 * MB;
+    if (bid < G) {
+        int hd = bid / MB;
+        gemm_body128<0, false, true>(As, Bs, vmsb + hd * 384, 2304,
+                                     WavT + (size_t)hd * 64 * 384, 384,
+                                     bav + hd * 64, nullptr, nullptr, attnb + hd * 64,
+                                     384, 384, (bid % MB) << 7, 0);
+    } else {
+        int b2 = bid - G;
+        gemm_body128<0, true, false>(As, Bs, tcb, 384, Wtp1T, 384, btp1, nullptr,
+                                     tcpf, nullptr, 192, 384,
+                                     (b2 / 3) << 7, (b2 % 3) << 6);
+    }
+}
+
+__global__ __launch_bounds__(256) void k_hs1(
+    const u16* __restrict__ A, const u16* __restrict__ BT,
+    const float* __restrict__ bias0, const float* __restrict__ bias1,
+    u16* __restrict__ Cb)
+{
+    __shared__ u16 As[128 * 72];
+    __shared__ u16 Bs[64 * 72];
+    gemm_body128<1, false, true>(As, Bs, A, 384, BT, 384, bias0, bias1,
+                                 nullptr, Cb, 768, 384,
+                                 blockIdx.y << 7, blockIdx.x << 6);
+}
+
+__global__ __launch_bounds__(256) void k_back(
+    const u16* __restrict__ hs1b, const u16* __restrict__ Wcp2T,
+    const float* __restrict__ bcp2, const float* __restrict__ anyv,
+    const float* __restrict__ fctx, float* __restrict__ outp,
+    const float* __restrict__ Wsw2, const float* __restrict__ bsw2,
+    float* __restrict__ swb, int MB, int BCc)
+{
+    __shared__ u16 As[128 * 72];
+    __shared__ u16 Bs[64 * 72];
+    int bid = blockIdx.x;
+    int G = 6 * MB;
+    if (bid < G) {
+        gemm_ctx_body(As, Bs, hs1b, Wcp2T, bcp2, anyv, fctx, outp,
+                      (bid / 6) << 7, (bid % 6) << 6);
+    } else {
+        int wid = (bid - G) * 4 + (threadIdx.x >> 6);
+        int lane = threadIdx.x & 63;
+        if (wid < BCc * 6) swb_wave(wid, lane, hs1b, Wsw2, bsw2, swb);
+    }
 }
 
 __global__ __launch_bounds__(384) void k_attnblk(
@@ -439,44 +541,40 @@
     u16* __restrict__ vmsb)
 {
     __shared__ u16 kvsb[32 * 392];
-    __shared__ u16 qSb[6 * 392];
     __shared__ u16 hidSb[32 * 200];
-    __shared__ u16 sdS[32 * 32];
     __shared__ float wsx[192];
-    __shared__ float bsS[32 * 8];
-    __shared__ float uSf[512];
-    u16* aS = (u16*)uSf;
-    float* sS = uSf;
+    __shared__ float bsS[256];
+    __shared__ float sS[256];
     const int b = blockIdx.x;
     const int t = threadIdx.x;
     const int lane = t & 63, wave = t >> 6;
     const int frm = lane & 15, frq = lane >> 4;
-    for (int i = t; i < 1152; i += 384) {
-        int h = i / 192, k2 = i - h * 192;
-        ((u32*)qSb)[h * 196 + k2] = ((const u32*)(Qpb + (size_t)b * 2304))[i];
-    }
+    const float* nr = nbr + (size_t)b * 960;
     {
-        const float* nr = nbr + (size_t)b * 960;
-        for (int i = t; i < 1024; i += 384) {
-            int r = i >> 5, cc = i & 31;
-            aS[r * 32 + cc] = (cc < 30) ? f2b(nr[r * 30 + cc]) : (u16)0;
-        }
-        if (t < 32) {
-            const float* nr2 = nr + t * 30;
-#pragma unroll
-            for (int s = 0; s < 6; s++) {
-                float qm = fs(qmask[b * 6 + s]);
-                sdS[t * 32 + s] = f2b((fs(qobs[b * 6 + s]) - nr2[s]) * qm);
-                sdS[t * 32 + 6 + s] = f2b(qm);
-            }
-#pragma unroll
-            for (int j = 12; j < 32; j++) sdS[t * 32 + j] = (u16)0;
-        }
-    }
-    __syncthreads();
-    {
-        bf16x8 a0 = *(const bf16x8*)&aS[frm * 32 + (frq << 3)];
-        bf16x8 a1 = *(const bf16x8*)&aS[(16 + frm) * 32 + (frq << 3)];
+        bf16x8 a0, a1, sa0, sa1;
+        float qm_[6], qo_[6];
+#pragma unroll
+        for (int s = 0; s < 6; s++) {
+            qm_[s] = fs(qmask[b * 6 + s]);
+            qo_[s] = fs(qobs[b * 6 + s]);
+        }
+#pragma unroll
+        for (int j = 0; j < 8; j++) {
+            int col = (frq << 3) + j;
+            float v0 = (col < 30) ? nr[frm * 30 + col] : 0.f;
+            float v1 = (col < 30) ? nr[(16 + frm) * 30 + col] : 0.f;
+            a0[j] = (short)f2b(v0);
+            a1[j] = (short)f2b(v1);
+            float s0, s1;
+            if (col < 6) {
+                s0 = (qo_[col] - nr[frm * 30 + col]) * qm_[col];
+                s1 = (qo_[col] - nr[(16 + frm) * 30 + col]) * qm_[col];
+            } else if (col < 12) {
+                s0 = qm_[col - 6]; s1 = qm_[col - 6];
+            } else { s0 = 0.f; s1 = 0.f; }
+            sa0[j] = (short)f2b(s0);
+            sa1[j] = (short)f2b(s1);
+        }
         const f32x4 z = {0.f, 0.f, 0.f, 0.f};
         f32x4 acc0[4] = {z, z, z, z};
         f32x4 acc1[4] = {z, z, z, z};
@@ -498,8 +596,6 @@
                 kvsb[(row0 + 16) * 392 + col] = f2b(gelu_f(acc1[ct][r] + bb));
             }
         }
-        bf16x8 sa0 = *(const bf16x8*)&sdS[frm * 32 + (frq << 3)];
-        bf16x8 sa1 = *(const bf16x8*)&sdS[(16 + frm) * 32 + (frq << 3)];
 #pragma unroll
         for (int ct = 0; ct < 2; ct++) {
             int col = (wave << 5) + (ct << 4) + frm;
@@ -517,12 +613,13 @@
     }
     __syncthreads();
     if (wave < 2) {
+        const u16* qp = Qpb + (size_t)b * 2304;
         f32x4 accs = {0.f, 0.f, 0.f, 0.f};
 #pragma unroll
         for (int ks = 0; ks < 12; ks++) {
             bf16x8 af = *(const bf16x8*)&kvsb[((wave << 4) + frm) * 392 + (ks << 5) + (frq << 3)];
             int hh = (frm < 6) ? frm : 0;
-            bf16x8 bf = *(const bf16x8*)&qSb[hh * 392 + (ks << 5) + (frq << 3)];
+            bf16x8 bf = *(const bf16x8*)&qp[hh * 384 + (ks << 5) + (frq << 3)];
             accs = __builtin_amdgcn_mfma_f32_16x16x32_bf16(af, bf, accs, 0, 0, 0);
         }
         if (frm < 6) {
@@ -587,24 +684,6 @@
         vp[1536 + t] = f2b(a4);
         vp[1920 + t] = f2b(a5);
     }
-}
-
-__global__ void k_swb_w(const u16* __restrict__ hs1b, const float* __restrict__ Wsw2,
-                        const float* __restrict__ bsw2, float* __restrict__ swb, int BCc)
-{
-    int wid = (blockIdx.x * 256 + threadIdx.x) >> 6;
-    int lane = threadIdx.x & 63;
-    if (wid >= BCc * 6) return;
-    int b = wid / 6, s = wid - b * 6;
-    float acc = 0.f;
-#pragma unroll
-    for (int i = 0; i < 6; i++) {
-        int n = lane + 64 * i;
-        acc += b2f(hs1b[(size_t)b * 768 + 384 + n]) * fs(Wsw2[n * 6 + s]);
-    }
-#pragma unroll
-    for (int m = 1; m <= 32; m <<= 1) acc += __shfl_xor(acc, m);
-    if (lane == 0) swb[b * 6 + s] = acc + fs(bsw2[s]);
 }
 
 __global__ void k_tail_w(const float* __restrict__ tcp, const float* __restrict__ pst,
@@ -809,30 +888,27 @@
     for (int c = 0; c < 4096 / BCc; c++) {
         const size_t B0 = (size_t)c * BCc;
         const int MB = BCc / 128;
-        const dim3 g6(6, MB), g3(3, MB), g12(12, MB), gao(6, MB);
-        const dim3 gqp(BCc / 64, 6);
-        k_prep L1(NBc)(i_rshift + B0 * 192, i_rsmask + B0 * 192, i_qcode + B0,
-                       i_rcodes + B0 * 32, i_rdist + B0 * 32, i_rc, i_Eres, nbr, NBc);
-        k_stats_w LW(BCc * 4)(nbr, i_rvalid + B0 * 32, pstf, gstf, anyf, BCc);
-        k_gemm_bb2<1><<<g12, 256, 0, stream>>>(
-            qeb + B0 * 512, 512, WqtqT, 512, i_bqp, i_btq, qtqb, 768, 512);
-        k_gemm_bb<0, false, true><<<g6, 256, 0, stream>>>(
-            qtqb, 768, WaqT, 384, i_baq, nullptr, Qhb, 384, 384);
-        k_qp_loop<<<gqp, 256, 0, stream>>>(Qhb, WakB, i_bak, Qpb, qkbf);
-        k_attnblk<<<BCc, 384, 0, stream>>>(nbr, WnpT, i_bnp, Qpb, qkbf,
-                                           i_qobs + B0 * 6, i_qmask + B0 * 6,
-                                           Wss1T, i_bss1, Wss2T, i_bss2,
-                                           i_rvalid + B0 * 32, anyf, vmsb);
-        k_attnout_bb<<<gao, 256, 0, stream>>>(vmsb, WavT, i_bav, attnb);
-        k_gemm_bb2<1><<<g12, 256, 0, stream>>>(
-            attnb, 384, Whs1T, 384, i_bcp1, i_bsw1, hs1b, 768, 384);
-        k_gemm_ctx<<<g6, 256, 0, stream>>>(
-            hs1b, 768, Wcp2T, 384, i_bcp2, anyf, i_fctx, out + B0 * 384, 384, 384);
-        k_swb_w LW(BCc * 6)(hs1b, i_Wsw2, i_bsw2, swbf, BCc);
-        k_gemm_tc<<<g6, 256, 0, stream>>>(
-            qtqb, i_qcode + B0, i_Etr, gstf, WtcT, i_btc, tcb);
-        k_gemm_bb<0, true, false><<<g3, 256, 0, stream>>>(
-            tcb, 384, Wtp1T, 384, i_btp1, tcpf, nullptr, 192, 384);
+        k_front<<<12 * MB + BCc / 8, 256, 0, stream>>>(
+            qeb + B0 * 512, WqtqT, i_bqp, i_btq, qtqb,
+            i_rshift + B0 * 192, i_rsmask + B0 * 192, i_qcode + B0,
+            i_rcodes + B0 * 32, i_rdist + B0 * 32, i_rc, i_Eres, nbr, MB, NBc);
+        k_mid<<<6 * MB + BCc, 256, 0, stream>>>(
+            qtqb, WaqT, i_baq, Qhb, nbr, i_rvalid + B0 * 32, pstf, gstf, anyf, MB, BCc);
+        k_qptc<<<(BCc / 64) * 6 + 6 * MB, 256, 0, stream>>>(
+            Qhb, WakB, i_bak, Qpb, qkbf,
+            qtqb, i_qcode + B0, i_Etr, gstf, WtcT, i_btc, tcb, BCc, MB);
+        k_attnblk<<<BCc, 384, 0, stream>>>(
+            nbr, WnpT, i_bnp, Qpb, qkbf, i_qobs + B0 * 6, i_qmask + B0 * 6,
+            Wss1T, i_bss1, Wss2T, i_bss2, i_rvalid + B0 * 32, anyf, vmsb);
+        k_aotp<<<9 * MB, 256, 0, stream>>>(
+            vmsb, WavT, i_bav, attnb, tcb, Wtp1T, i_btp1, tcpf, MB);
+        {
+            dim3 g12(12, MB);
+            k_hs1<<<g12, 256, 0, stream>>>(attnb, Whs1T, i_bcp1, i_bsw1, hs1b);
+        }
+        k_back<<<6 * MB + (BCc * 3) / 2, 256, 0, stream>>>(
+            hs1b, Wcp2T, i_bcp2, anyf, i_fctx, out + B0 * 384,
+            i_Wsw2, i_bsw2, swbf, MB, BCc);
         k_tail_w LW(BCc * 9)(tcpf, pstf, i_Wtp1, i_Wtp2, i_btp2,
                              out + (size_t)4096 * 390 + B0 * 6,
                              nbr, i_rsmask + B0 * 192, i_rvalid + B0 * 32, swbf, anyf,
```

Result: slower. 403.0 us (+2.2%).
